# Kernel tuning notes

Hardware: AMD Instinct MI355X
Metric: run time of the kernel (lower is better)

## Reference

```python
import jax, jax.numpy as jnp
import numpy as np

P = 2        # patch size (all 3 dims)
NB = 8       # num_bands
N = 16       # d_state
DTR = 8      # dt_rank = d_model // 16
DCONV = 4    # d_conv
SMAX = 2.0   # smax_dt = smax_B = smax_C


def _ln(x, g, b):
    mu = x.mean(-1, keepdims=True)
    v = ((x - mu) ** 2).mean(-1, keepdims=True)
    return (x - mu) / jnp.sqrt(v + 1e-5) * g + b


def _silu(x):
    return x * jax.nn.sigmoid(x)


def _ssm_layer(x, band, m, rho, Win, bin_, convw, convb, Wx, Wdt, bdt, Alog, Dp,
               Wout, bout, edt, eB, eC, wr, wm):
    # x: [B, L, d_model] -> bidirectional conditioned selective scan (BiFCSSM)
    Bsz, L, _ = x.shape
    ED = convw.shape[0]
    xz = x @ Win + bin_
    xp, z = xz[..., :ED], xz[..., ED:]
    # depthwise causal conv1d over L
    xpad = jnp.pad(xp, ((0, 0), (DCONV - 1, 0), (0, 0)))
    xc = sum(xpad[:, k:k + L, :] * convw[:, k] for k in range(DCONV)) + convb
    xc = _silu(xc)
    dbl = xc @ Wx                                    # [B,L,DTR+2N]
    dt = jax.nn.softplus(dbl[..., :DTR] @ Wdt + bdt)  # [B,L,ED]
    # band/radius/mask conditioned modulation of delta, B, C
    s_dt = SMAX * jax.nn.sigmoid(edt[band][None] + wr[0] * rho[None] + wm[0] * m)
    s_B = SMAX * jax.nn.sigmoid(eB[band][None] + wr[1] * rho[None] + wm[1] * m)
    s_C = SMAX * jax.nn.sigmoid(eC[band][None] + wr[2] * rho[None] + wm[2] * m)
    dt = dt * s_dt[..., None]
    Bm = dbl[..., DTR:DTR + N] * s_B[..., None]       # [B,L,N]
    Cm = dbl[..., DTR + N:] * s_C[..., None]          # [B,L,N]
    A = -jnp.exp(Alog)                                # [ED,N]
    dA = jnp.exp(dt[..., None] * A)                   # [B,L,ED,N]
    dBu = (dA - 1.0) / A * Bm[:, :, None, :] * xc[..., None]   # exact ZOH
    dA_s = jnp.moveaxis(dA, 1, 0)
    dBu_s = jnp.moveaxis(dBu, 1, 0)
    C_s = jnp.moveaxis(Cm, 1, 0)
    h0 = jnp.zeros((Bsz, ED, N), x.dtype)

    def step(h, inp):
        a, bu, c = inp
        h = a * h + bu
        return h, jnp.einsum('ben,bn->be', h, c)

    _, yf = jax.lax.scan(step, h0, (dA_s, dBu_s, C_s))
    _, yb = jax.lax.scan(step, h0, (dA_s, dBu_s, C_s), reverse=True)
    y = jnp.moveaxis(yf + yb, 0, 1) + Dp * xc
    y = y * _silu(z)
    return y @ Wout + bout


def _fwd(kspace_ri, mask, pe_w, pe_b, pu_w, pu_b, ln_g, ln_b, fn_g, fn_b,
         cond_band, cond_rad_w, cond_mask_w, l0_Win, l0_bin, l0_convw, l0_convb,
         l0_Wx, l0_Wdt, l0_bdt, l0_Alog, l0_D, l0_Wout, l0_bout, l0_edt, l0_eB,
         l0_eC, l0_wr, l0_wm):
    Bsz, C, nx, ny, nz = kspace_ri.shape
    gx, gy, gz = nx // P, ny // P, nz // P
    L = gx * gy * gz
    # patch embed (Conv3d, kernel==stride) as blocked einsum
    xr = kspace_ri.reshape(Bsz, C, gx, P, gy, P, gz, P)
    x = jnp.einsum('bcxiyjzk,dcijk->bdxyz', xr, pe_w) + pe_b[None, :, None, None, None]
    DM = x.shape[1]
    x = x.reshape(Bsz, DM, L).transpose(0, 2, 1)               # [B,L,D]
    m = mask.reshape(Bsz, 1, gx, P, gy, P, gz, P).mean(axis=(3, 5, 7)).reshape(Bsz, L)
    m = jnp.clip(m, 0.0, 1.0)
    # raster scan ordering: identity permutation, rho_bar, band ids
    rho = jnp.arange(L, dtype=x.dtype) / float(L - 1)
    band = jnp.clip(jnp.floor(rho * NB).astype(jnp.int32), 0, NB - 1)
    # condition tokens
    cond = cond_band[band][None] + rho[None, :, None] * cond_rad_w + m[:, :, None] * cond_mask_w
    h = _ln(x + cond, ln_g, ln_b)
    h = h + _ssm_layer(_ln(h, fn_g, fn_b), band, m, rho, l0_Win, l0_bin, l0_convw,
                       l0_convb, l0_Wx, l0_Wdt, l0_bdt, l0_Alog, l0_D, l0_Wout,
                       l0_bout, l0_edt, l0_eB, l0_eC, l0_wr, l0_wm)
    # patch unembed (ConvTranspose3d, kernel==stride) as blocked einsum
    hg = h.transpose(0, 2, 1).reshape(Bsz, DM, gx, gy, gz)
    out = jnp.einsum('bdxyz,dcijk->bcxiyjzk', hg, pu_w).reshape(Bsz, C, nx, ny, nz)
    out = out + pu_b[None, :, None, None, None]
    return kspace_ri + out


def setup_inputs() -> dict:
    key = jax.random.key(0)
    ks = jax.random.split(key, 24)
    ED, DM, CIN = 256, 128, 16

    def nrm(k, shape, s):
        return jax.random.normal(k, shape, jnp.float32) * s

    return {
        'kspace_ri': jax.random.normal(ks[0], (1, CIN, 64, 64, 16), jnp.float32),
        'mask': jax.random.uniform(ks[1], (1, 1, 64, 64, 16), jnp.float32),
        'pe_w': nrm(ks[2], (DM, CIN, P, P, P), 0.09),
        'pe_b': nrm(ks[3], (DM,), 0.02),
        'pu_w': nrm(ks[4], (DM, CIN, P, P, P), 0.05),
        'pu_b': jnp.zeros((CIN,), jnp.float32),
        'ln_g': jnp.ones((DM,), jnp.float32),
        'ln_b': jnp.zeros((DM,), jnp.float32),
        'fn_g': jnp.ones((DM,), jnp.float32),
        'fn_b': jnp.zeros((DM,), jnp.float32),
        'cond_band': nrm(ks[5], (NB, DM), 0.02),
        'cond_rad_w': nrm(ks[6], (DM,), 0.02),
        'cond_mask_w': nrm(ks[7], (DM,), 0.02),
        'l0_Win': nrm(ks[8], (DM, 2 * ED), 0.05),
        'l0_bin': jnp.zeros((2 * ED,), jnp.float32),
        'l0_convw': nrm(ks[9], (ED, DCONV), 0.2),
        'l0_convb': jnp.zeros((ED,), jnp.float32),
        'l0_Wx': nrm(ks[10], (ED, DTR + 2 * N), 0.05),
        'l0_Wdt': nrm(ks[11], (DTR, ED), 0.1),
        'l0_bdt': jnp.full((ED,), -3.0, jnp.float32),
        'l0_Alog': jnp.log(jnp.tile(jnp.arange(1, N + 1, dtype=jnp.float32), (ED, 1))),
        'l0_D': jnp.ones((ED,), jnp.float32),
        'l0_Wout': nrm(ks[12], (ED, DM), 0.05),
        'l0_bout': jnp.zeros((DM,), jnp.float32),
        'l0_edt': nrm(ks[13], (NB,), 0.1),
        'l0_eB': nrm(ks[14], (NB,), 0.1),
        'l0_eC': nrm(ks[15], (NB,), 0.1),
        'l0_wr': nrm(ks[16], (3,), 0.1),
        'l0_wm': nrm(ks[17], (3,), 0.1),
    }


def reference(kspace_ri, mask, pe_w, pe_b, pu_w, pu_b, ln_g, ln_b, fn_g, fn_b,
              cond_band, cond_rad_w, cond_mask_w, l0_Win, l0_bin, l0_convw,
              l0_convb, l0_Wx, l0_Wdt, l0_bdt, l0_Alog, l0_D, l0_Wout, l0_bout,
              l0_edt, l0_eB, l0_eC, l0_wr, l0_wm):
    return _fwd(kspace_ri, mask, pe_w, pe_b, pu_w, pu_b, ln_g, ln_b, fn_g, fn_b,
                cond_band, cond_rad_w, cond_mask_w, l0_Win, l0_bin, l0_convw,
                l0_convb, l0_Wx, l0_Wdt, l0_bdt, l0_Alog, l0_D, l0_Wout, l0_bout,
                l0_edt, l0_eB, l0_eC, l0_wr, l0_wm)
```

## Files before the change

### kernel.cpp

```cpp
#include <hip/hip_runtime.h>
#include <hip/hip_bf16.h>

#define L_TOK 8192
#define NCh 256
#define CLh 32
#define LOG2E 1.44269504088896f

typedef short bf16x8 __attribute__((ext_vector_type(8)));
typedef float f32x4 __attribute__((ext_vector_type(4)));

static __device__ __forceinline__ float nexp2(float x) {
#if __has_builtin(__builtin_amdgcn_exp2f)
    return __builtin_amdgcn_exp2f(x);
#else
    return exp2f(x);
#endif
}
static __device__ __forceinline__ float sigm(float x) {
    return 1.f / (1.f + nexp2(-x * LOG2E));
}
static __device__ __forceinline__ ushort f2bf(float x) {
    union { float f; uint u; } v; v.f = x;
    uint r = v.u + 0x7fffu + ((v.u >> 16) & 1u);
    return (ushort)(r >> 16);
}
static __device__ __forceinline__ float bf2f(ushort h) {
    union { float f; uint u; } v; v.u = ((uint)h) << 16;
    return v.f;
}
static __device__ __forceinline__ void f2hl(float x, ushort* hi, ushort* lo) {
    ushort h = f2bf(x);
    *hi = h;
    *lo = f2bf(x - bf2f(h));
}

#define W_PE   0
#define W_WIN  16384
#define W_WOUT 81920
#define W_PU   114688
#define W_PROJ 131072
#define W_TOT  212992

__global__ __launch_bounds__(256) void prep_k(const float* __restrict__ pe_w, const float* __restrict__ Win,
                                              const float* __restrict__ Wx, const float* __restrict__ Wdt,
                                              const float* __restrict__ Wout, const float* __restrict__ pu_w,
                                              const float* __restrict__ mask,
                                              ushort* __restrict__ wH, ushort* __restrict__ wL,
                                              float* __restrict__ mbuf) {
    int b = blockIdx.x;
    if (b >= 832) {
        int l = (b - 832) * 256 + threadIdx.x;
        int xg = l >> 8, yg = (l >> 3) & 31, zg = l & 7;
        float s = 0.f;
        for (int i2 = 0; i2 < 2; ++i2)
            for (int j2 = 0; j2 < 2; ++j2)
                for (int k2 = 0; k2 < 2; ++k2)
                    s += mask[(2 * xg + i2) * 1024 + (2 * yg + j2) * 16 + 2 * zg + k2];
        s *= 0.125f;
        mbuf[l] = fminf(fmaxf(s, 0.f), 1.f);
        return;
    }
    int i = b * 256 + threadIdx.x;
    float v;
    if (i < 16384) {
        v = pe_w[i];
    } else if (i < 81920) {
        int j = i - 16384; int n = j >> 7, k = j & 127;
        v = Win[k * 512 + n];
    } else if (i < 114688) {
        int j = i - 81920; int n = j >> 8, k = j & 255;
        v = Wout[k * 128 + n];
    } else if (i < 131072) {
        int j = i - 114688; int n = j >> 7, k = j & 127;
        v = pu_w[k * 128 + n];
    } else {
        int j = i - 131072; int n = j >> 8, k = j & 255;
        if (n < 256) {
            float s = 0.f;
#pragma unroll
            for (int r = 0; r < 8; ++r) s += Wx[k * 40 + r] * Wdt[r * 256 + n];
            v = s;
        } else if (n < 288) {
            v = Wx[k * 40 + 8 + (n - 256)];
        } else {
            v = 0.f;
        }
    }
    ushort h, lo; f2hl(v, &h, &lo);
    wH[i] = h; wL[i] = lo;
}

__global__ __launch_bounds__(256) void embed_ln_k(const float* __restrict__ ks,
                                                  const ushort* __restrict__ wH, const ushort* __restrict__ wL,
                                                  const float* __restrict__ pe_b, const float* __restrict__ cond_band,
                                                  const float* __restrict__ cond_rad, const float* __restrict__ cond_mask,
                                                  const float* __restrict__ mbuf,
                                                  const float* __restrict__ ln_g, const float* __restrict__ ln_b,
                                                  const float* __restrict__ fn_g, const float* __restrict__ fn_b,
                                                  float* __restrict__ h_,
                                                  ushort* __restrict__ hnH, ushort* __restrict__ hnL) {
    __shared__ __align__(16) char smem[41472];
    ushort (*AsH)[72] = (ushort(*)[72])(smem);
    ushort (*AsL)[72] = (ushort(*)[72])(smem + 2304);
    ushort (*BsH)[72] = (ushort(*)[72])(smem + 4608);
    ushort (*BsL)[72] = (ushort(*)[72])(smem + 23040);
    float  (*Cs)[132] = (float(*)[132])(smem);

    const int tid = threadIdx.x;
    const int lane = tid & 63, wn = tid >> 6;
    const int ln = lane & 15, q = lane >> 4;
    const int mb = blockIdx.x * 16;

    f32x4 acc[2];
    acc[0] = (f32x4){0.f, 0.f, 0.f, 0.f};
    acc[1] = (f32x4){0.f, 0.f, 0.f, 0.f};

    for (int kc = 0; kc < 128; kc += 64) {
        __syncthreads();
        for (int u = tid; u < 1024; u += 256) {
            int r = u >> 6, kk = u & 63;
            int l = mb + r, k = kc + kk;
            int cc = k >> 3, ijk = k & 7;
            int xg = l >> 8, yg = (l >> 3) & 31, zg = l & 7;
            int i2 = (ijk >> 2) & 1, j2 = (ijk >> 1) & 1, k2 = ijk & 1;
            float v = ks[cc * 65536 + (2 * xg + i2) * 1024 + (2 * yg + j2) * 16 + 2 * zg + k2];
            ushort h, lo; f2hl(v, &h, &lo);
            AsH[r][kk] = h; AsL[r][kk] = lo;
        }
        for (int u = tid; u < 1024; u += 256) {
            int n = u >> 3, g = u & 7;
            *(uint4*)&BsH[n][g * 8] = *(const uint4*)&wH[W_PE + n * 128 + kc + g * 8];
            *(uint4*)&BsL[n][g * 8] = *(const uint4*)&wL[W_PE + n * 128 + kc + g * 8];
        }
        __syncthreads();
#pragma unroll
        for (int ks_ = 0; ks_ < 64; ks_ += 32) {
            const int kk = ks_ + q * 8;
            bf16x8 ah = *(const bf16x8*)&AsH[ln][kk];
            bf16x8 al = *(const bf16x8*)&AsL[ln][kk];
#pragma unroll
            for (int cb = 0; cb < 2; ++cb) {
                bf16x8 bh = *(const bf16x8*)&BsH[wn * 32 + cb * 16 + ln][kk];
                bf16x8 bl = *(const bf16x8*)&BsL[wn * 32 + cb * 16 + ln][kk];
                acc[cb] = __builtin_amdgcn_mfma_f32_16x16x32_bf16(ah, bh, acc[cb], 0, 0, 0);
                acc[cb] = __builtin_amdgcn_mfma_f32_16x16x32_bf16(ah, bl, acc[cb], 0, 0, 0);
                acc[cb] = __builtin_amdgcn_mfma_f32_16x16x32_bf16(al, bh, acc[cb], 0, 0, 0);
            }
        }
    }
    __syncthreads();
#pragma unroll
    for (int cb = 0; cb < 2; ++cb) {
#pragma unroll
        for (int r = 0; r < 4; ++r) {
            int row = q * 4 + r;
            int col = wn * 32 + cb * 16 + ln;
            int l = mb + row;
            float rho = (float)l * (1.0f / 8191.0f);
            int band = min(7, (int)(rho * 8.0f));
            Cs[row][col] = acc[cb][r] + pe_b[col] + cond_band[band * 128 + col]
                           + rho * cond_rad[col] + mbuf[l] * cond_mask[col];
        }
    }
    __syncthreads();
    {
        int row = tid >> 4, j = tid & 15;
        int l = mb + row;
        float v8[8];
        float s = 0.f, s2 = 0.f;
#pragma unroll
        for (int i = 0; i < 8; ++i) {
            float v = Cs[row][j * 8 + i];
            v8[i] = v; s += v; s2 += v * v;
        }
#pragma unroll
        for (int o = 1; o < 16; o <<= 1) { s += __shfl_xor(s, o, 16); s2 += __shfl_xor(s2, o, 16); }
        float mu = s * (1.f / 128.f);
        float var = s2 * (1.f / 128.f) - mu * mu;
        float rstd = rsqrtf(fmaxf(var, 0.f) + 1e-5f);
        float hv[8];
        s = 0.f; s2 = 0.f;
#pragma unroll
        for (int i = 0; i < 8; ++i) {
            int col = j * 8 + i;
            float h = (v8[i] - mu) * rstd * ln_g[col] + ln_b[col];
            hv[i] = h; s += h; s2 += h * h;
        }
#pragma unroll
        for (int i = 0; i < 8; i += 4)
            *(float4*)&h_[(size_t)l * 128 + j * 8 + i] = make_float4(hv[i], hv[i + 1], hv[i + 2], hv[i + 3]);
#pragma unroll
        for (int o = 1; o < 16; o <<= 1) { s += __shfl_xor(s, o, 16); s2 += __shfl_xor(s2, o, 16); }
        mu = s * (1.f / 128.f);
        var = s2 * (1.f / 128.f) - mu * mu;
        rstd = rsqrtf(fmaxf(var, 0.f) + 1e-5f);
        union { ushort u[8]; uint4 v4; } oh, ol;
#pragma unroll
        for (int i = 0; i < 8; ++i) {
            int col = j * 8 + i;
            float o2 = (hv[i] - mu) * rstd * fn_g[col] + fn_b[col];
            ushort hh, ll; f2hl(o2, &hh, &ll);
            oh.u[i] = hh; ol.u[i] = ll;
        }
        *(uint4*)&hnH[(size_t)l * 128 + j * 8] = oh.v4;
        *(uint4*)&hnL[(size_t)l * 128 + j * 8] = ol.v4;
    }
}

__global__ __launch_bounds__(256) void win_k(const ushort* __restrict__ Ah, const ushort* __restrict__ Al,
                                             const ushort* __restrict__ wH, const ushort* __restrict__ wL,
                                             const float* __restrict__ bin_,
                                             float* __restrict__ xp, float* __restrict__ sz) {
    __shared__ ushort AsH[64][72], AsL[64][72];
    __shared__ ushort BsH[64][72], BsL[64][72];
    const int tid = threadIdx.x;
    const int lane = tid & 63, wave = tid >> 6;
    const int wm = wave & 1, wn = wave >> 1;
    const int ln = lane & 15, q = lane >> 4;
    const int mb = blockIdx.x * 64, nb = blockIdx.y * 64;

    f32x4 acc[2][2];
#pragma unroll
    for (int rb = 0; rb < 2; ++rb)
#pragma unroll
        for (int cb = 0; cb < 2; ++cb) acc[rb][cb] = (f32x4){0.f, 0.f, 0.f, 0.f};

    for (int kc = 0; kc < 128; kc += 64) {
        __syncthreads();
        for (int u = tid; u < 512; u += 256) {
            int r = u >> 3, g = u & 7;
            size_t go = (size_t)(mb + r) * 128 + kc + g * 8;
            *(uint4*)&AsH[r][g * 8] = *(const uint4*)&Ah[go];
            *(uint4*)&AsL[r][g * 8] = *(const uint4*)&Al[go];
        }
        for (int u = tid; u < 512; u += 256) {
            int n = u >> 3, g = u & 7;
            size_t go = (size_t)(W_WIN) + (size_t)(nb + n) * 128 + kc + g * 8;
            *(uint4*)&BsH[n][g * 8] = *(const uint4*)&wH[go];
            *(uint4*)&BsL[n][g * 8] = *(const uint4*)&wL[go];
        }
        __syncthreads();
#pragma unroll
        for (int ks_ = 0; ks_ < 64; ks_ += 32) {
            const int kk = ks_ + q * 8;
            bf16x8 ah[2], al[2], bh[2], bl[2];
#pragma unroll
            for (int rb = 0; rb < 2; ++rb) {
                ah[rb] = *(const bf16x8*)&AsH[wm * 32 + rb * 16 + ln][kk];
                al[rb] = *(const bf16x8*)&AsL[wm * 32 + rb * 16 + ln][kk];
            }
#pragma unroll
            for (int cb = 0; cb < 2; ++cb) {
                bh[cb] = *(const bf16x8*)&BsH[wn * 32 + cb * 16 + ln][kk];
                bl[cb] = *(const bf16x8*)&BsL[wn * 32 + cb * 16 + ln][kk];
            }
#pragma unroll
            for (int rb = 0; rb < 2; ++rb)
#pragma unroll
                for (int cb = 0; cb < 2; ++cb) {
                    acc[rb][cb] = __builtin_amdgcn_mfma_f32_16x16x32_bf16(ah[rb], bh[cb], acc[rb][cb], 0, 0, 0);
                    acc[rb][cb] = __builtin_amdgcn_mfma_f32_16x16x32_bf16(ah[rb], bl[cb], acc[rb][cb], 0, 0, 0);
                    acc[rb][cb] = __builtin_amdgcn_mfma_f32_16x16x32_bf16(al[rb], bh[cb], acc[rb][cb], 0, 0, 0);
                }
        }
    }
#pragma unroll
    for (int rb = 0; rb < 2; ++rb)
#pragma unroll
        for (int cb = 0; cb < 2; ++cb)
#pragma unroll
            for (int r = 0; r < 4; ++r) {
                int l = mb + wm * 32 + rb * 16 + q * 4 + r;
                int col = nb + wn * 32 + cb * 16 + ln;
                float v = acc[rb][cb][r] + bin_[col];
                if (col < 256) {
                    xp[(size_t)l * 256 + col] = v;
                } else {
                    sz[(size_t)l * 256 + (col - 256)] = v * sigm(v);
                }
            }
}

__global__ __launch_bounds__(256) void conv_k(const float* __restrict__ xp, const float* __restrict__ convw,
                                              const float* __restrict__ convb, float* __restrict__ xc) {
    int id = blockIdx.x * 256 + threadIdx.x;
    int l = id >> 6, e4 = (id & 63) * 4;
    float4 cw[4];
#pragma unroll
    for (int j = 0; j < 4; ++j) cw[j] = *(const float4*)&convw[(e4 + j) * 4];
    float4 cb = *(const float4*)&convb[e4];
    float o[4] = {cb.x, cb.y, cb.z, cb.w};
#pragma unroll
    for (int k = 0; k < 4; ++k) {
        int lp = l - 3 + k;
        if (lp >= 0) {
            float4 t = *(const float4*)&xp[(size_t)lp * 256 + e4];
            o[0] += t.x * ((const float*)&cw[0])[k];
            o[1] += t.y * ((const float*)&cw[1])[k];
            o[2] += t.z * ((const float*)&cw[2])[k];
            o[3] += t.w * ((const float*)&cw[3])[k];
        }
    }
    float4 r;
    r.x = o[0] * sigm(o[0]);
    r.y = o[1] * sigm(o[1]);
    r.z = o[2] * sigm(o[2]);
    r.w = o[3] * sigm(o[3]);
    *(float4*)&xc[(size_t)l * 256 + e4] = r;
}

__global__ __launch_bounds__(256) void proj_k(const float* __restrict__ xc,
                                              const ushort* __restrict__ wH, const ushort* __restrict__ wL,
                                              const float* __restrict__ bdt, const float* __restrict__ mbuf,
                                              const float* __restrict__ edt, const float* __restrict__ eB,
                                              const float* __restrict__ eC, const float* __restrict__ wr,
                                              const float* __restrict__ wm,
                                              float* __restrict__ dt, float* __restrict__ Bm, float* __restrict__ Cm) {
    __shared__ ushort AsH[64][72], AsL[64][72];
    __shared__ ushort BsH[64][72], BsL[64][72];
    const int tid = threadIdx.x;
    const int lane = tid & 63, wave = tid >> 6;
    const int wm_ = wave & 1, wn = wave >> 1;
    const int ln = lane & 15, q = lane >> 4;
    const int mb = blockIdx.x * 64, nb = blockIdx.y * 64;

    f32x4 acc[2][2];
#pragma unroll
    for (int rb = 0; rb < 2; ++rb)
#pragma unroll
        for (int cb = 0; cb < 2; ++cb) acc[rb][cb] = (f32x4){0.f, 0.f, 0.f, 0.f};

    for (int kc = 0; kc < 256; kc += 64) {
        __syncthreads();
        for (int u = tid; u < 1024; u += 256) {
            int r = u >> 4, kq = u & 15;
            float4 v = *(const float4*)&xc[(size_t)(mb + r) * 256 + kc + kq * 4];
            union { ushort u[4]; uint2 v2; } hh, ll;
            f2hl(v.x, &hh.u[0], &ll.u[0]); f2hl(v.y, &hh.u[1], &ll.u[1]);
            f2hl(v.z, &hh.u[2], &ll.u[2]); f2hl(v.w, &hh.u[3], &ll.u[3]);
            *(uint2*)&AsH[r][kq * 4] = hh.v2;
            *(uint2*)&AsL[r][kq * 4] = ll.v2;
        }
        for (int u = tid; u < 512; u += 256) {
            int n = u >> 3, g = u & 7;
            size_t go = (size_t)(W_PROJ) + (size_t)(nb + n) * 256 + kc + g * 8;
            *(uint4*)&BsH[n][g * 8] = *(const uint4*)&wH[go];
            *(uint4*)&BsL[n][g * 8] = *(const uint4*)&wL[go];
        }
        __syncthreads();
#pragma unroll
        for (int ks_ = 0; ks_ < 64; ks_ += 32) {
            const int kk = ks_ + q * 8;
            bf16x8 ah[2], al[2], bh[2], bl[2];
#pragma unroll
            for (int rb = 0; rb < 2; ++rb) {
                ah[rb] = *(const bf16x8*)&AsH[wm_ * 32 + rb * 16 + ln][kk];
                al[rb] = *(const bf16x8*)&AsL[wm_ * 32 + rb * 16 + ln][kk];
            }
#pragma unroll
            for (int cb = 0; cb < 2; ++cb) {
                bh[cb] = *(const bf16x8*)&BsH[wn * 32 + cb * 16 + ln][kk];
                bl[cb] = *(const bf16x8*)&BsL[wn * 32 + cb * 16 + ln][kk];
            }
#pragma unroll
            for (int rb = 0; rb < 2; ++rb)
#pragma unroll
                for (int cb = 0; cb < 2; ++cb) {
                    acc[rb][cb] = __builtin_amdgcn_mfma_f32_16x16x32_bf16(ah[rb], bh[cb], acc[rb][cb], 0, 0, 0);
                    acc[rb][cb] = __builtin_amdgcn_mfma_f32_16x16x32_bf16(ah[rb], bl[cb], acc[rb][cb], 0, 0, 0);
                    acc[rb][cb] = __builtin_amdgcn_mfma_f32_16x16x32_bf16(al[rb], bh[cb], acc[rb][cb], 0, 0, 0);
                }
        }
    }
#pragma unroll
    for (int rb = 0; rb < 2; ++rb)
#pragma unroll
        for (int cb = 0; cb < 2; ++cb)
#pragma unroll
            for (int r = 0; r < 4; ++r) {
                int l = mb + wm_ * 32 + rb * 16 + q * 4 + r;
                int col = nb + wn * 32 + cb * 16 + ln;
                float v = acc[rb][cb][r];
                float rho = (float)l * (1.0f / 8191.0f);
                int band = min(7, (int)(rho * 8.0f));
                float mv = mbuf[l];
                if (col < 256) {
                    float sc0 = 2.0f * sigm(edt[band] + wr[0] * rho + wm[0] * mv);
                    float v2 = v + bdt[col];
                    float sp = (v2 > 20.f) ? v2 : log1pf(expf(v2));
                    dt[(size_t)l * 256 + col] = sp * sc0;
                } else if (col < 272) {
                    float sc1 = 2.0f * sigm(eB[band] + wr[1] * rho + wm[1] * mv);
                    Bm[(size_t)l * 16 + (col - 256)] = v * sc1;
                } else if (col < 288) {
                    float sc2 = 2.0f * sigm(eC[band] + wr[2] * rho + wm[2] * mv);
                    Cm[(size_t)l * 16 + (col - 272)] = v * sc2;
                }
            }
}

__global__ __launch_bounds__(256) void scan0_k(const float* __restrict__ dt, const float* __restrict__ xc,
                                               const float* __restrict__ Bm, const float* __restrict__ Alog,
                                               float* __restrict__ Hb, float* __restrict__ sdtb) {
    const int c = blockIdx.x, dir = blockIdx.y, e = threadIdx.x;
    __shared__ float bms[CLh][16];
    for (int idx = e; idx < CLh * 16; idx += 256)
        bms[idx >> 4][idx & 15] = Bm[c * (CLh * 16) + idx];
    float A2[16], iv[16], h[16];
#pragma unroll
    for (int n = 0; n < 16; ++n) {
        float ea = nexp2(Alog[e * 16 + n] * LOG2E);
        A2[n] = -ea * LOG2E;
        iv[n] = -1.0f / ea;
        h[n] = 0.f;
    }
    const int base = c * CLh;
    float cu[8], cx[8], nu[8], nx[8];
#pragma unroll
    for (int j = 0; j < 8; ++j) {
        int p = dir ? (CLh - 1 - j) : j;
        cu[j] = dt[(size_t)(base + p) * 256 + e];
        cx[j] = xc[(size_t)(base + p) * 256 + e];
    }
    __syncthreads();
    float sdt = 0.f;
#pragma unroll
    for (int g = 0; g < CLh / 8; ++g) {
        if (g + 1 < CLh / 8) {
#pragma unroll
            for (int j = 0; j < 8; ++j) {
                int s = (g + 1) * 8 + j;
                int p = dir ? (CLh - 1 - s) : s;
                nu[j] = dt[(size_t)(base + p) * 256 + e];
                nx[j] = xc[(size_t)(base + p) * 256 + e];
            }
        }
#pragma unroll
        for (int j = 0; j < 8; ++j) {
            int s = g * 8 + j;
            int p = dir ? (CLh - 1 - s) : s;
            float u = cu[j], xv = cx[j];
            union { float4 v[4]; float f[16]; } bb;
            const float4* bp = (const float4*)&bms[p][0];
            bb.v[0] = bp[0]; bb.v[1] = bp[1]; bb.v[2] = bp[2]; bb.v[3] = bp[3];
#pragma unroll
            for (int n = 0; n < 16; ++n) {
                float a = nexp2(A2[n] * u);
                float w = xv * bb.f[n] * iv[n];
                h[n] = a * (h[n] + w) - w;
            }
            sdt += u;
        }
#pragma unroll
        for (int j = 0; j < 8; ++j) { cu[j] = nu[j]; cx[j] = nx[j]; }
    }
    const size_t hofs = (size_t)(dir * NCh + c) * 4096 + e * 16;
#pragma unroll
    for (int j = 0; j < 4; ++j)
        *(float4*)&Hb[hofs + 4 * j] = make_float4(h[4 * j], h[4 * j + 1], h[4 * j + 2], h[4 * j + 3]);
    if (dir == 0) sdtb[c * 256 + e] = sdt;
}

__global__ __launch_bounds__(64) void combine_k(const float* __restrict__ Hb, float* __restrict__ Hpre,
                                                const float* __restrict__ sdtb, const float* __restrict__ Alog) {
    int id = blockIdx.x * 64 + threadIdx.x;
    int dir = id >> 12, en = id & 4095, e = en >> 4;
    float A2 = -nexp2(Alog[en] * LOG2E) * LOG2E;
    float hi = 0.f;
    for (int g = 0; g < NCh / 8; ++g) {
        float Pv[8], qv[8];
#pragma unroll
        for (int j = 0; j < 8; ++j) {
            int c = dir ? (NCh - 1 - (g * 8 + j)) : (g * 8 + j);
            Pv[j] = sdtb[c * 256 + e];
            qv[j] = Hb[(size_t)(dir * NCh + c) * 4096 + en];
        }
#pragma unroll
        for (int j = 0; j < 8; ++j) {
            int c = dir ? (NCh - 1 - (g * 8 + j)) : (g * 8 + j);
            float P = nexp2(A2 * Pv[j]);
            Hpre[(size_t)(dir * NCh + c) * 4096 + en] = hi;
            hi = P * hi + qv[j];
        }
    }
}

template <int DIR>
static __device__ __forceinline__ void scan_dir(const float* __restrict__ dt, const float* __restrict__ xc,
                                                int base, int e,
                                                const float (*bms)[16], const float (*cms)[16],
                                                const float* A2, const float* iv,
                                                float* h, float* yreg) {
    float cu[8], cx[8], nu[8], nx[8];
#pragma unroll
    for (int j = 0; j < 8; ++j) {
        const int p = DIR ? (CLh - 1 - j) : j;
        cu[j] = dt[(size_t)(base + p) * 256 + e];
        cx[j] = xc[(size_t)(base + p) * 256 + e];
    }
#pragma unroll
    for (int g = 0; g < CLh / 8; ++g) {
        if (g + 1 < CLh / 8) {
#pragma unroll
            for (int j = 0; j < 8; ++j) {
                const int s = (g + 1) * 8 + j;
                const int p = DIR ? (CLh - 1 - s) : s;
                nu[j] = dt[(size_t)(base + p) * 256 + e];
                nx[j] = xc[(size_t)(base + p) * 256 + e];
            }
        }
#pragma unroll
        for (int j = 0; j < 8; ++j) {
            const int s = g * 8 + j;
            const int p = DIR ? (CLh - 1 - s) : s;
            float u = cu[j], xv = cx[j];
            union { float4 v[4]; float f[16]; } bb, cc;
            const float4* bp = (const float4*)&bms[p][0];
            bb.v[0] = bp[0]; bb.v[1] = bp[1]; bb.v[2] = bp[2]; bb.v[3] = bp[3];
            const float4* cp = (const float4*)&cms[p][0];
            cc.v[0] = cp[0]; cc.v[1] = cp[1]; cc.v[2] = cp[2]; cc.v[3] = cp[3];
            float y = 0.f;
#pragma unroll
            for (int n = 0; n < 16; ++n) {
                float a = nexp2(A2[n] * u);
                float w = xv * bb.f[n] * iv[n];
                h[n] = a * (h[n] + w) - w;
                y += h[n] * cc.f[n];
            }
            yreg[p] = y;
        }
#pragma unroll
        for (int j = 0; j < 8; ++j) { cu[j] = nu[j]; cx[j] = nx[j]; }
    }
}

__global__ __launch_bounds__(512) void scan1g_k(const float* __restrict__ dt, const float* __restrict__ xc,
                                                const float* __restrict__ Bm, const float* __restrict__ Cm,
                                                const float* __restrict__ Alog, const float* __restrict__ Hpre,
                                                const float* __restrict__ sz, const float* __restrict__ Dp,
                                                ushort* __restrict__ AHo, ushort* __restrict__ ALo) {
    const int c = blockIdx.x;
    const int tid = threadIdx.x;
    const int dir = tid >> 8;
    const int e = tid & 255;
    __shared__ float bms[CLh][16];
    __shared__ float cms[CLh][16];
    __shared__ float ysum[CLh][256];
    for (int idx = tid; idx < CLh * 16; idx += 512) {
        bms[idx >> 4][idx & 15] = Bm[c * (CLh * 16) + idx];
        cms[idx >> 4][idx & 15] = Cm[c * (CLh * 16) + idx];
    }
    float A2[16], iv[16], h[16];
#pragma unroll
    for (int n = 0; n < 16; ++n) {
        float ea = nexp2(Alog[e * 16 + n] * LOG2E);
        A2[n] = -ea * LOG2E;
        iv[n] = -1.0f / ea;
    }
    const size_t hofs = (size_t)(dir * NCh + c) * 4096 + e * 16;
#pragma unroll
    for (int j = 0; j < 4; ++j) {
        float4 hv = *(const float4*)&Hpre[hofs + 4 * j];
        h[4 * j] = hv.x; h[4 * j + 1] = hv.y; h[4 * j + 2] = hv.z; h[4 * j + 3] = hv.w;
    }
    const int base = c * CLh;
    float yreg[CLh];
    __syncthreads();
    if (dir == 0) {
        scan_dir<0>(dt, xc, base, e, bms, cms, A2, iv, h, yreg);
    } else {
        scan_dir<1>(dt, xc, base, e, bms, cms, A2, iv, h, yreg);
    }
    __syncthreads();
    if (dir == 0) {
#pragma unroll
        for (int l = 0; l < CLh; ++l) ysum[l][e] = yreg[l];
    }
    __syncthreads();
    if (dir == 1) {
        float dpv = Dp[e];
#pragma unroll
        for (int l = 0; l < CLh; ++l) {
            size_t gl = (size_t)(base + l) * 256 + e;
            float a = (ysum[l][e] + yreg[l] + dpv * xc[gl]) * sz[gl];
            ushort hh, ll; f2hl(a, &hh, &ll);
            AHo[gl] = hh; ALo[gl] = ll;
        }
    }
}

__global__ __launch_bounds__(256) void wout_k(const ushort* __restrict__ AH, const ushort* __restrict__ AL,
                                              const ushort* __restrict__ wH, const ushort* __restrict__ wL,
                                              const float* __restrict__ bout, const float* __restrict__ h_,
                                              ushort* __restrict__ hfH, ushort* __restrict__ hfL) {
    __shared__ ushort AsH[32][72], AsL[32][72];
    __shared__ ushort BsH[64][72], BsL[64][72];
    const int tid = threadIdx.x;
    const int lane = tid & 63, wave = tid >> 6;
    const int wm = wave & 1, wn = wave >> 1;
    const int ln = lane & 15, q = lane >> 4;
    const int mb = blockIdx.x * 32, nb = blockIdx.y * 64;

    f32x4 acc[2];
    acc[0] = (f32x4){0.f, 0.f, 0.f, 0.f};
    acc[1] = (f32x4){0.f, 0.f, 0.f, 0.f};

    for (int kc = 0; kc < 256; kc += 64) {
        __syncthreads();
        for (int u = tid; u < 256; u += 256) {
            int r = u >> 3, g = u & 7;
            size_t go = (size_t)(mb + r) * 256 + kc + g * 8;
            *(uint4*)&AsH[r][g * 8] = *(const uint4*)&AH[go];
            *(uint4*)&AsL[r][g * 8] = *(const uint4*)&AL[go];
        }
        for (int u = tid; u < 512; u += 256) {
            int n = u >> 3, g = u & 7;
            size_t go = (size_t)(W_WOUT) + (size_t)(nb + n) * 256 + kc + g * 8;
            *(uint4*)&BsH[n][g * 8] = *(const uint4*)&wH[go];
            *(uint4*)&BsL[n][g * 8] = *(const uint4*)&wL[go];
        }
        __syncthreads();
#pragma unroll
        for (int ks_ = 0; ks_ < 64; ks_ += 32) {
            const int kk = ks_ + q * 8;
            bf16x8 ah = *(const bf16x8*)&AsH[wm * 16 + ln][kk];
            bf16x8 al = *(const bf16x8*)&AsL[wm * 16 + ln][kk];
#pragma unroll
            for (int cb = 0; cb < 2; ++cb) {
                bf16x8 bh = *(const bf16x8*)&BsH[wn * 32 + cb * 16 + ln][kk];
                bf16x8 bl = *(const bf16x8*)&BsL[wn * 32 + cb * 16 + ln][kk];
                acc[cb] = __builtin_amdgcn_mfma_f32_16x16x32_bf16(ah, bh, acc[cb], 0, 0, 0);
                acc[cb] = __builtin_amdgcn_mfma_f32_16x16x32_bf16(ah, bl, acc[cb], 0, 0, 0);
                acc[cb] = __builtin_amdgcn_mfma_f32_16x16x32_bf16(al, bh, acc[cb], 0, 0, 0);
            }
        }
    }
#pragma unroll
    for (int cb = 0; cb < 2; ++cb)
#pragma unroll
        for (int r = 0; r < 4; ++r) {
            int l = mb + wm * 16 + q * 4 + r;
            int col = nb + wn * 32 + cb * 16 + ln;
            float v = acc[cb][r] + bout[col] + h_[(size_t)l * 128 + col];
            ushort hh, ll; f2hl(v, &hh, &ll);
            hfH[(size_t)l * 128 + col] = hh;
            hfL[(size_t)l * 128 + col] = ll;
        }
}

__global__ __launch_bounds__(256) void unembed_k(const ushort* __restrict__ Ah, const ushort* __restrict__ Al,
                                                 const ushort* __restrict__ wH, const ushort* __restrict__ wL,
                                                 const float* __restrict__ pu_b, const float* __restrict__ ks,
                                                 float* __restrict__ out) {
    __shared__ ushort AsH[32][72], AsL[32][72];
    __shared__ ushort BsH[64][72], BsL[64][72];
    const int tid = threadIdx.x;
    const int lane = tid & 63, wave = tid >> 6;
    const int wm = wave & 1, wn = wave >> 1;
    const int ln = lane & 15, q = lane >> 4;
    const int mb = blockIdx.x * 32, nb = blockIdx.y * 64;

    f32x4 acc[2];
    acc[0] = (f32x4){0.f, 0.f, 0.f, 0.f};
    acc[1] = (f32x4){0.f, 0.f, 0.f, 0.f};

    for (int kc = 0; kc < 128; kc += 64) {
        __syncthreads();
        for (int u = tid; u < 256; u += 256) {
            int r = u >> 3, g = u & 7;
            size_t go = (size_t)(mb + r) * 128 + kc + g * 8;
            *(uint4*)&AsH[r][g * 8] = *(const uint4*)&Ah[go];
            *(uint4*)&AsL[r][g * 8] = *(const uint4*)&Al[go];
        }
        for (int u = tid; u < 512; u += 256) {
            int n = u >> 3, g = u & 7;
            size_t go = (size_t)(W_PU) + (size_t)(nb + n) * 128 + kc + g * 8;
            *(uint4*)&BsH[n][g * 8] = *(const uint4*)&wH[go];
            *(uint4*)&BsL[n][g * 8] = *(const uint4*)&wL[go];
        }
        __syncthreads();
#pragma unroll
        for (int ks_ = 0; ks_ < 64; ks_ += 32) {
            const int kk = ks_ + q * 8;
            bf16x8 ah = *(const bf16x8*)&AsH[wm * 16 + ln][kk];
            bf16x8 al = *(const bf16x8*)&AsL[wm * 16 + ln][kk];
#pragma unroll
            for (int cb = 0; cb < 2; ++cb) {
                bf16x8 bh = *(const bf16x8*)&BsH[wn * 32 + cb * 16 + ln][kk];
                bf16x8 bl = *(const bf16x8*)&BsL[wn * 32 + cb * 16 + ln][kk];
                acc[cb] = __builtin_amdgcn_mfma_f32_16x16x32_bf16(ah, bh, acc[cb], 0, 0, 0);
                acc[cb] = __builtin_amdgcn_mfma_f32_16x16x32_bf16(ah, bl, acc[cb], 0, 0, 0);
                acc[cb] = __builtin_amdgcn_mfma_f32_16x16x32_bf16(al, bh, acc[cb], 0, 0, 0);
            }
        }
    }
#pragma unroll
    for (int cb = 0; cb < 2; ++cb)
#pragma unroll
        for (int r = 0; r < 4; ++r) {
            int l = mb + wm * 16 + q * 4 + r;
            int col = nb + wn * 32 + cb * 16 + ln;
            int xg = l >> 8, yg = (l >> 3) & 31, zg = l & 7;
            int c = col >> 3, ijk = col & 7;
            int i2 = (ijk >> 2) & 1, j2 = (ijk >> 1) & 1, k2 = ijk & 1;
            size_t idx = (size_t)((c * 64 + 2 * xg + i2) * 64 + (2 * yg + j2)) * 16 + 2 * zg + k2;
            out[idx] = acc[cb][r] + pu_b[c] + ks[idx];
        }
}

extern "C" void kernel_launch(void* const* d_in, const int* in_sizes, int n_in,
                              void* d_out, int out_size, void* d_ws, size_t ws_size,
                              hipStream_t stream) {
    const float* ks    = (const float*)d_in[0];
    const float* mask  = (const float*)d_in[1];
    const float* pe_w  = (const float*)d_in[2];
    const float* pe_b  = (const float*)d_in[3];
    const float* pu_w  = (const float*)d_in[4];
    const float* pu_b  = (const float*)d_in[5];
    const float* ln_g  = (const float*)d_in[6];
    const float* ln_b  = (const float*)d_in[7];
    const float* fn_g  = (const float*)d_in[8];
    const float* fn_b  = (const float*)d_in[9];
    const float* cond_band = (const float*)d_in[10];
    const float* cond_rad  = (const float*)d_in[11];
    const float* cond_mask = (const float*)d_in[12];
    const float* Win   = (const float*)d_in[13];
    const float* bin_  = (const float*)d_in[14];
    const float* convw = (const float*)d_in[15];
    const float* convb = (const float*)d_in[16];
    const float* Wx    = (const float*)d_in[17];
    const float* Wdt   = (const float*)d_in[18];
    const float* bdt   = (const float*)d_in[19];
    const float* Alog  = (const float*)d_in[20];
    const float* Dp    = (const float*)d_in[21];
    const float* Wout  = (const float*)d_in[22];
    const float* bout  = (const float*)d_in[23];
    const float* edt   = (const float*)d_in[24];
    const float* eB    = (const float*)d_in[25];
    const float* eC    = (const float*)d_in[26];
    const float* wr    = (const float*)d_in[27];
    const float* wm    = (const float*)d_in[28];
    float* out = (float*)d_out;

    char* base = (char*)d_ws;
    size_t o = 0;
    auto alloc = [&](size_t bytes) { char* p = base + o; o += (bytes + 255) & ~(size_t)255; return p; };
    float*  mbuf = (float*)alloc(32768);
    ushort* wH   = (ushort*)alloc(W_TOT * 2);
    ushort* wL   = (ushort*)alloc(W_TOT * 2);
    float*  h_   = (float*)alloc(4194304);
    ushort* hnH  = (ushort*)alloc(2097152);
    ushort* hnL  = (ushort*)alloc(2097152);
    float*  xp   = (float*)alloc(8388608);
    float*  sz   = (float*)alloc(8388608);
    float*  xc   = (float*)alloc(8388608);
    float*  dt   = (float*)alloc(8388608);
    float*  Bm   = (float*)alloc(524288);
    float*  Cm   = (float*)alloc(524288);
    float*  Hb   = (float*)alloc(8388608);
    float*  Hpre = (float*)alloc(8388608);
    float*  sdtb = (float*)alloc(262144);
    ushort* AHo  = (ushort*)alloc(4194304);
    ushort* ALo  = (ushort*)alloc(4194304);
    ushort* hfH  = (ushort*)alloc(2097152);
    ushort* hfL  = (ushort*)alloc(2097152);

    prep_k<<<864, 256, 0, stream>>>(pe_w, Win, Wx, Wdt, Wout, pu_w, mask, wH, wL, mbuf);
    embed_ln_k<<<512, 256, 0, stream>>>(ks, wH, wL, pe_b, cond_band, cond_rad, cond_mask, mbuf,
                                        ln_g, ln_b, fn_g, fn_b, h_, hnH, hnL);
    win_k<<<dim3(128, 8), 256, 0, stream>>>(hnH, hnL, wH, wL, bin_, xp, sz);
    conv_k<<<2048, 256, 0, stream>>>(xp, convw, convb, xc);
    proj_k<<<dim3(128, 5), 256, 0, stream>>>(xc, wH, wL, bdt, mbuf, edt, eB, eC, wr, wm, dt, Bm, Cm);
    scan0_k<<<dim3(NCh, 2), 256, 0, stream>>>(dt, xc, Bm, Alog, Hb, sdtb);
    combine_k<<<128, 64, 0, stream>>>(Hb, Hpre, sdtb, Alog);
    scan1g_k<<<NCh, 512, 0, stream>>>(dt, xc, Bm, Cm, Alog, Hpre, sz, Dp, AHo, ALo);
    wout_k<<<dim3(256, 2), 256, 0, stream>>>(AHo, ALo, wH, wL, bout, h_, hfH, hfL);
    unembed_k<<<dim3(256, 2), 256, 0, stream>>>(hfH, hfL, wH, wL, pu_b, ks, out);
}
```

Measured before the change: 240.0 us.

## Fuse all pipeline stages into one cooperative persistent megakernel with grid syncs

Replaces the ten separate kernel launches (prep, embed+LN, in-projection, conv, projection, two-pass chunked scan, combine, out-projection, unembed) with a single cooperative kernel of 256 blocks × 512 threads that separates stages with grid-wide syncs. The aim is to remove per-launch overhead and inter-kernel gaps. In exchange, every stage is forced onto a fixed 256-block, 512-thread configuration, which may lower occupancy or parallelism for stages that previously used larger grids. Grid syncs also add their own barrier cost.

```diff
diff --git a/kernel.cpp b/kernel.cpp
--- a/kernel.cpp
+++ b/kernel.cpp
@@ -1,7 +1,8 @@
 #include <hip/hip_runtime.h>
 #include <hip/hip_bf16.h>
-
-#define L_TOK 8192
+#include <hip/hip_cooperative_groups.h>
+namespace cg = cooperative_groups;
+
 #define NCh 256
 #define CLh 32
 #define LOG2E 1.44269504088896f
@@ -41,449 +42,17 @@
 #define W_PROJ 131072
 #define W_TOT  212992
 
-__global__ __launch_bounds__(256) void prep_k(const float* __restrict__ pe_w, const float* __restrict__ Win,
-                                              const float* __restrict__ Wx, const float* __restrict__ Wdt,
-                                              const float* __restrict__ Wout, const float* __restrict__ pu_w,
-                                              const float* __restrict__ mask,
-                                              ushort* __restrict__ wH, ushort* __restrict__ wL,
-                                              float* __restrict__ mbuf) {
-    int b = blockIdx.x;
-    if (b >= 832) {
-        int l = (b - 832) * 256 + threadIdx.x;
-        int xg = l >> 8, yg = (l >> 3) & 31, zg = l & 7;
-        float s = 0.f;
-        for (int i2 = 0; i2 < 2; ++i2)
-            for (int j2 = 0; j2 < 2; ++j2)
-                for (int k2 = 0; k2 < 2; ++k2)
-                    s += mask[(2 * xg + i2) * 1024 + (2 * yg + j2) * 16 + 2 * zg + k2];
-        s *= 0.125f;
-        mbuf[l] = fminf(fmaxf(s, 0.f), 1.f);
-        return;
-    }
-    int i = b * 256 + threadIdx.x;
-    float v;
-    if (i < 16384) {
-        v = pe_w[i];
-    } else if (i < 81920) {
-        int j = i - 16384; int n = j >> 7, k = j & 127;
-        v = Win[k * 512 + n];
-    } else if (i < 114688) {
-        int j = i - 81920; int n = j >> 8, k = j & 255;
-        v = Wout[k * 128 + n];
-    } else if (i < 131072) {
-        int j = i - 114688; int n = j >> 7, k = j & 127;
-        v = pu_w[k * 128 + n];
-    } else {
-        int j = i - 131072; int n = j >> 8, k = j & 255;
-        if (n < 256) {
-            float s = 0.f;
-#pragma unroll
-            for (int r = 0; r < 8; ++r) s += Wx[k * 40 + r] * Wdt[r * 256 + n];
-            v = s;
-        } else if (n < 288) {
-            v = Wx[k * 40 + 8 + (n - 256)];
-        } else {
-            v = 0.f;
-        }
-    }
-    ushort h, lo; f2hl(v, &h, &lo);
-    wH[i] = h; wL[i] = lo;
-}
-
-__global__ __launch_bounds__(256) void embed_ln_k(const float* __restrict__ ks,
-                                                  const ushort* __restrict__ wH, const ushort* __restrict__ wL,
-                                                  const float* __restrict__ pe_b, const float* __restrict__ cond_band,
-                                                  const float* __restrict__ cond_rad, const float* __restrict__ cond_mask,
-                                                  const float* __restrict__ mbuf,
-                                                  const float* __restrict__ ln_g, const float* __restrict__ ln_b,
-                                                  const float* __restrict__ fn_g, const float* __restrict__ fn_b,
-                                                  float* __restrict__ h_,
-                                                  ushort* __restrict__ hnH, ushort* __restrict__ hnL) {
-    __shared__ __align__(16) char smem[41472];
-    ushort (*AsH)[72] = (ushort(*)[72])(smem);
-    ushort (*AsL)[72] = (ushort(*)[72])(smem + 2304);
-    ushort (*BsH)[72] = (ushort(*)[72])(smem + 4608);
-    ushort (*BsL)[72] = (ushort(*)[72])(smem + 23040);
-    float  (*Cs)[132] = (float(*)[132])(smem);
-
-    const int tid = threadIdx.x;
-    const int lane = tid & 63, wn = tid >> 6;
-    const int ln = lane & 15, q = lane >> 4;
-    const int mb = blockIdx.x * 16;
-
-    f32x4 acc[2];
-    acc[0] = (f32x4){0.f, 0.f, 0.f, 0.f};
-    acc[1] = (f32x4){0.f, 0.f, 0.f, 0.f};
-
-    for (int kc = 0; kc < 128; kc += 64) {
-        __syncthreads();
-        for (int u = tid; u < 1024; u += 256) {
-            int r = u >> 6, kk = u & 63;
-            int l = mb + r, k = kc + kk;
-            int cc = k >> 3, ijk = k & 7;
-            int xg = l >> 8, yg = (l >> 3) & 31, zg = l & 7;
-            int i2 = (ijk >> 2) & 1, j2 = (ijk >> 1) & 1, k2 = ijk & 1;
-            float v = ks[cc * 65536 + (2 * xg + i2) * 1024 + (2 * yg + j2) * 16 + 2 * zg + k2];
-            ushort h, lo; f2hl(v, &h, &lo);
-            AsH[r][kk] = h; AsL[r][kk] = lo;
-        }
-        for (int u = tid; u < 1024; u += 256) {
-            int n = u >> 3, g = u & 7;
-            *(uint4*)&BsH[n][g * 8] = *(const uint4*)&wH[W_PE + n * 128 + kc + g * 8];
-            *(uint4*)&BsL[n][g * 8] = *(const uint4*)&wL[W_PE + n * 128 + kc + g * 8];
-        }
-        __syncthreads();
-#pragma unroll
-        for (int ks_ = 0; ks_ < 64; ks_ += 32) {
-            const int kk = ks_ + q * 8;
-            bf16x8 ah = *(const bf16x8*)&AsH[ln][kk];
-            bf16x8 al = *(const bf16x8*)&AsL[ln][kk];
-#pragma unroll
-            for (int cb = 0; cb < 2; ++cb) {
-                bf16x8 bh = *(const bf16x8*)&BsH[wn * 32 + cb * 16 + ln][kk];
-                bf16x8 bl = *(const bf16x8*)&BsL[wn * 32 + cb * 16 + ln][kk];
-                acc[cb] = __builtin_amdgcn_mfma_f32_16x16x32_bf16(ah, bh, acc[cb], 0, 0, 0);
-                acc[cb] = __builtin_amdgcn_mfma_f32_16x16x32_bf16(ah, bl, acc[cb], 0, 0, 0);
-                acc[cb] = __builtin_amdgcn_mfma_f32_16x16x32_bf16(al, bh, acc[cb], 0, 0, 0);
-            }
-        }
-    }
-    __syncthreads();
-#pragma unroll
-    for (int cb = 0; cb < 2; ++cb) {
-#pragma unroll
-        for (int r = 0; r < 4; ++r) {
-            int row = q * 4 + r;
-            int col = wn * 32 + cb * 16 + ln;
-            int l = mb + row;
-            float rho = (float)l * (1.0f / 8191.0f);
-            int band = min(7, (int)(rho * 8.0f));
-            Cs[row][col] = acc[cb][r] + pe_b[col] + cond_band[band * 128 + col]
-                           + rho * cond_rad[col] + mbuf[l] * cond_mask[col];
-        }
-    }
-    __syncthreads();
-    {
-        int row = tid >> 4, j = tid & 15;
-        int l = mb + row;
-        float v8[8];
-        float s = 0.f, s2 = 0.f;
-#pragma unroll
-        for (int i = 0; i < 8; ++i) {
-            float v = Cs[row][j * 8 + i];
-            v8[i] = v; s += v; s2 += v * v;
-        }
-#pragma unroll
-        for (int o = 1; o < 16; o <<= 1) { s += __shfl_xor(s, o, 16); s2 += __shfl_xor(s2, o, 16); }
-        float mu = s * (1.f / 128.f);
-        float var = s2 * (1.f / 128.f) - mu * mu;
-        float rstd = rsqrtf(fmaxf(var, 0.f) + 1e-5f);
-        float hv[8];
-        s = 0.f; s2 = 0.f;
-#pragma unroll
-        for (int i = 0; i < 8; ++i) {
-            int col = j * 8 + i;
-            float h = (v8[i] - mu) * rstd * ln_g[col] + ln_b[col];
-            hv[i] = h; s += h; s2 += h * h;
-        }
-#pragma unroll
-        for (int i = 0; i < 8; i += 4)
-            *(float4*)&h_[(size_t)l * 128 + j * 8 + i] = make_float4(hv[i], hv[i + 1], hv[i + 2], hv[i + 3]);
-#pragma unroll
-        for (int o = 1; o < 16; o <<= 1) { s += __shfl_xor(s, o, 16); s2 += __shfl_xor(s2, o, 16); }
-        mu = s * (1.f / 128.f);
-        var = s2 * (1.f / 128.f) - mu * mu;
-        rstd = rsqrtf(fmaxf(var, 0.f) + 1e-5f);
-        union { ushort u[8]; uint4 v4; } oh, ol;
-#pragma unroll
-        for (int i = 0; i < 8; ++i) {
-            int col = j * 8 + i;
-            float o2 = (hv[i] - mu) * rstd * fn_g[col] + fn_b[col];
-            ushort hh, ll; f2hl(o2, &hh, &ll);
-            oh.u[i] = hh; ol.u[i] = ll;
-        }
-        *(uint4*)&hnH[(size_t)l * 128 + j * 8] = oh.v4;
-        *(uint4*)&hnL[(size_t)l * 128 + j * 8] = ol.v4;
-    }
-}
-
-__global__ __launch_bounds__(256) void win_k(const ushort* __restrict__ Ah, const ushort* __restrict__ Al,
-                                             const ushort* __restrict__ wH, const ushort* __restrict__ wL,
-                                             const float* __restrict__ bin_,
-                                             float* __restrict__ xp, float* __restrict__ sz) {
-    __shared__ ushort AsH[64][72], AsL[64][72];
-    __shared__ ushort BsH[64][72], BsL[64][72];
-    const int tid = threadIdx.x;
-    const int lane = tid & 63, wave = tid >> 6;
-    const int wm = wave & 1, wn = wave >> 1;
-    const int ln = lane & 15, q = lane >> 4;
-    const int mb = blockIdx.x * 64, nb = blockIdx.y * 64;
-
-    f32x4 acc[2][2];
-#pragma unroll
-    for (int rb = 0; rb < 2; ++rb)
-#pragma unroll
-        for (int cb = 0; cb < 2; ++cb) acc[rb][cb] = (f32x4){0.f, 0.f, 0.f, 0.f};
-
-    for (int kc = 0; kc < 128; kc += 64) {
-        __syncthreads();
-        for (int u = tid; u < 512; u += 256) {
-            int r = u >> 3, g = u & 7;
-            size_t go = (size_t)(mb + r) * 128 + kc + g * 8;
-            *(uint4*)&AsH[r][g * 8] = *(const uint4*)&Ah[go];
-            *(uint4*)&AsL[r][g * 8] = *(const uint4*)&Al[go];
-        }
-        for (int u = tid; u < 512; u += 256) {
-            int n = u >> 3, g = u & 7;
-            size_t go = (size_t)(W_WIN) + (size_t)(nb + n) * 128 + kc + g * 8;
-            *(uint4*)&BsH[n][g * 8] = *(const uint4*)&wH[go];
-            *(uint4*)&BsL[n][g * 8] = *(const uint4*)&wL[go];
-        }
-        __syncthreads();
-#pragma unroll
-        for (int ks_ = 0; ks_ < 64; ks_ += 32) {
-            const int kk = ks_ + q * 8;
-            bf16x8 ah[2], al[2], bh[2], bl[2];
-#pragma unroll
-            for (int rb = 0; rb < 2; ++rb) {
-                ah[rb] = *(const bf16x8*)&AsH[wm * 32 + rb * 16 + ln][kk];
-                al[rb] = *(const bf16x8*)&AsL[wm * 32 + rb * 16 + ln][kk];
-            }
-#pragma unroll
-            for (int cb = 0; cb < 2; ++cb) {
-                bh[cb] = *(const bf16x8*)&BsH[wn * 32 + cb * 16 + ln][kk];
-                bl[cb] = *(const bf16x8*)&BsL[wn * 32 + cb * 16 + ln][kk];
-            }
-#pragma unroll
-            for (int rb = 0; rb < 2; ++rb)
-#pragma unroll
-                for (int cb = 0; cb < 2; ++cb) {
-                    acc[rb][cb] = __builtin_amdgcn_mfma_f32_16x16x32_bf16(ah[rb], bh[cb], acc[rb][cb], 0, 0, 0);
-                    acc[rb][cb] = __builtin_amdgcn_mfma_f32_16x16x32_bf16(ah[rb], bl[cb], acc[rb][cb], 0, 0, 0);
-                    acc[rb][cb] = __builtin_amdgcn_mfma_f32_16x16x32_bf16(al[rb], bh[cb], acc[rb][cb], 0, 0, 0);
-                }
-        }
-    }
-#pragma unroll
-    for (int rb = 0; rb < 2; ++rb)
-#pragma unroll
-        for (int cb = 0; cb < 2; ++cb)
-#pragma unroll
-            for (int r = 0; r < 4; ++r) {
-                int l = mb + wm * 32 + rb * 16 + q * 4 + r;
-                int col = nb + wn * 32 + cb * 16 + ln;
-                float v = acc[rb][cb][r] + bin_[col];
-                if (col < 256) {
-                    xp[(size_t)l * 256 + col] = v;
-                } else {
-                    sz[(size_t)l * 256 + (col - 256)] = v * sigm(v);
-                }
-            }
-}
-
-__global__ __launch_bounds__(256) void conv_k(const float* __restrict__ xp, const float* __restrict__ convw,
-                                              const float* __restrict__ convb, float* __restrict__ xc) {
-    int id = blockIdx.x * 256 + threadIdx.x;
-    int l = id >> 6, e4 = (id & 63) * 4;
-    float4 cw[4];
-#pragma unroll
-    for (int j = 0; j < 4; ++j) cw[j] = *(const float4*)&convw[(e4 + j) * 4];
-    float4 cb = *(const float4*)&convb[e4];
-    float o[4] = {cb.x, cb.y, cb.z, cb.w};
-#pragma unroll
-    for (int k = 0; k < 4; ++k) {
-        int lp = l - 3 + k;
-        if (lp >= 0) {
-            float4 t = *(const float4*)&xp[(size_t)lp * 256 + e4];
-            o[0] += t.x * ((const float*)&cw[0])[k];
-            o[1] += t.y * ((const float*)&cw[1])[k];
-            o[2] += t.z * ((const float*)&cw[2])[k];
-            o[3] += t.w * ((const float*)&cw[3])[k];
-        }
-    }
-    float4 r;
-    r.x = o[0] * sigm(o[0]);
-    r.y = o[1] * sigm(o[1]);
-    r.z = o[2] * sigm(o[2]);
-    r.w = o[3] * sigm(o[3]);
-    *(float4*)&xc[(size_t)l * 256 + e4] = r;
-}
-
-__global__ __launch_bounds__(256) void proj_k(const float* __restrict__ xc,
-                                              const ushort* __restrict__ wH, const ushort* __restrict__ wL,
-                                              const float* __restrict__ bdt, const float* __restrict__ mbuf,
-                                              const float* __restrict__ edt, const float* __restrict__ eB,
-                                              const float* __restrict__ eC, const float* __restrict__ wr,
-                                              const float* __restrict__ wm,
-                                              float* __restrict__ dt, float* __restrict__ Bm, float* __restrict__ Cm) {
-    __shared__ ushort AsH[64][72], AsL[64][72];
-    __shared__ ushort BsH[64][72], BsL[64][72];
-    const int tid = threadIdx.x;
-    const int lane = tid & 63, wave = tid >> 6;
-    const int wm_ = wave & 1, wn = wave >> 1;
-    const int ln = lane & 15, q = lane >> 4;
-    const int mb = blockIdx.x * 64, nb = blockIdx.y * 64;
-
-    f32x4 acc[2][2];
-#pragma unroll
-    for (int rb = 0; rb < 2; ++rb)
-#pragma unroll
-        for (int cb = 0; cb < 2; ++cb) acc[rb][cb] = (f32x4){0.f, 0.f, 0.f, 0.f};
-
-    for (int kc = 0; kc < 256; kc += 64) {
-        __syncthreads();
-        for (int u = tid; u < 1024; u += 256) {
-            int r = u >> 4, kq = u & 15;
-            float4 v = *(const float4*)&xc[(size_t)(mb + r) * 256 + kc + kq * 4];
-            union { ushort u[4]; uint2 v2; } hh, ll;
-            f2hl(v.x, &hh.u[0], &ll.u[0]); f2hl(v.y, &hh.u[1], &ll.u[1]);
-            f2hl(v.z, &hh.u[2], &ll.u[2]); f2hl(v.w, &hh.u[3], &ll.u[3]);
-            *(uint2*)&AsH[r][kq * 4] = hh.v2;
-            *(uint2*)&AsL[r][kq * 4] = ll.v2;
-        }
-        for (int u = tid; u < 512; u += 256) {
-            int n = u >> 3, g = u & 7;
-            size_t go = (size_t)(W_PROJ) + (size_t)(nb + n) * 256 + kc + g * 8;
-            *(uint4*)&BsH[n][g * 8] = *(const uint4*)&wH[go];
-            *(uint4*)&BsL[n][g * 8] = *(const uint4*)&wL[go];
-        }
-        __syncthreads();
-#pragma unroll
-        for (int ks_ = 0; ks_ < 64; ks_ += 32) {
-            const int kk = ks_ + q * 8;
-            bf16x8 ah[2], al[2], bh[2], bl[2];
-#pragma unroll
-            for (int rb = 0; rb < 2; ++rb) {
-                ah[rb] = *(const bf16x8*)&AsH[wm_ * 32 + rb * 16 + ln][kk];
-                al[rb] = *(const bf16x8*)&AsL[wm_ * 32 + rb * 16 + ln][kk];
-            }
-#pragma unroll
-            for (int cb = 0; cb < 2; ++cb) {
-                bh[cb] = *(const bf16x8*)&BsH[wn * 32 + cb * 16 + ln][kk];
-                bl[cb] = *(const bf16x8*)&BsL[wn * 32 + cb * 16 + ln][kk];
-            }
-#pragma unroll
-            for (int rb = 0; rb < 2; ++rb)
-#pragma unroll
-                for (int cb = 0; cb < 2; ++cb) {
-                    acc[rb][cb] = __builtin_amdgcn_mfma_f32_16x16x32_bf16(ah[rb], bh[cb], acc[rb][cb], 0, 0, 0);
-                    acc[rb][cb] = __builtin_amdgcn_mfma_f32_16x16x32_bf16(ah[rb], bl[cb], acc[rb][cb], 0, 0, 0);
-                    acc[rb][cb] = __builtin_amdgcn_mfma_f32_16x16x32_bf16(al[rb], bh[cb], acc[rb][cb], 0, 0, 0);
-                }
-        }
-    }
-#pragma unroll
-    for (int rb = 0; rb < 2; ++rb)
-#pragma unroll
-        for (int cb = 0; cb < 2; ++cb)
-#pragma unroll
-            for (int r = 0; r < 4; ++r) {
-                int l = mb + wm_ * 32 + rb * 16 + q * 4 + r;
-                int col = nb + wn * 32 + cb * 16 + ln;
-                float v = acc[rb][cb][r];
-                float rho = (float)l * (1.0f / 8191.0f);
-                int band = min(7, (int)(rho * 8.0f));
-                float mv = mbuf[l];
-                if (col < 256) {
-                    float sc0 = 2.0f * sigm(edt[band] + wr[0] * rho + wm[0] * mv);
-                    float v2 = v + bdt[col];
-                    float sp = (v2 > 20.f) ? v2 : log1pf(expf(v2));
-                    dt[(size_t)l * 256 + col] = sp * sc0;
-                } else if (col < 272) {
-                    float sc1 = 2.0f * sigm(eB[band] + wr[1] * rho + wm[1] * mv);
-                    Bm[(size_t)l * 16 + (col - 256)] = v * sc1;
-                } else if (col < 288) {
-                    float sc2 = 2.0f * sigm(eC[band] + wr[2] * rho + wm[2] * mv);
-                    Cm[(size_t)l * 16 + (col - 272)] = v * sc2;
-                }
-            }
-}
-
-__global__ __launch_bounds__(256) void scan0_k(const float* __restrict__ dt, const float* __restrict__ xc,
-                                               const float* __restrict__ Bm, const float* __restrict__ Alog,
-                                               float* __restrict__ Hb, float* __restrict__ sdtb) {
-    const int c = blockIdx.x, dir = blockIdx.y, e = threadIdx.x;
-    __shared__ float bms[CLh][16];
-    for (int idx = e; idx < CLh * 16; idx += 256)
-        bms[idx >> 4][idx & 15] = Bm[c * (CLh * 16) + idx];
-    float A2[16], iv[16], h[16];
-#pragma unroll
-    for (int n = 0; n < 16; ++n) {
-        float ea = nexp2(Alog[e * 16 + n] * LOG2E);
-        A2[n] = -ea * LOG2E;
-        iv[n] = -1.0f / ea;
-        h[n] = 0.f;
-    }
-    const int base = c * CLh;
-    float cu[8], cx[8], nu[8], nx[8];
-#pragma unroll
-    for (int j = 0; j < 8; ++j) {
-        int p = dir ? (CLh - 1 - j) : j;
-        cu[j] = dt[(size_t)(base + p) * 256 + e];
-        cx[j] = xc[(size_t)(base + p) * 256 + e];
-    }
-    __syncthreads();
-    float sdt = 0.f;
-#pragma unroll
-    for (int g = 0; g < CLh / 8; ++g) {
-        if (g + 1 < CLh / 8) {
-#pragma unroll
-            for (int j = 0; j < 8; ++j) {
-                int s = (g + 1) * 8 + j;
-                int p = dir ? (CLh - 1 - s) : s;
-                nu[j] = dt[(size_t)(base + p) * 256 + e];
-                nx[j] = xc[(size_t)(base + p) * 256 + e];
-            }
-        }
-#pragma unroll
-        for (int j = 0; j < 8; ++j) {
-            int s = g * 8 + j;
-            int p = dir ? (CLh - 1 - s) : s;
-            float u = cu[j], xv = cx[j];
-            union { float4 v[4]; float f[16]; } bb;
-            const float4* bp = (const float4*)&bms[p][0];
-            bb.v[0] = bp[0]; bb.v[1] = bp[1]; bb.v[2] = bp[2]; bb.v[3] = bp[3];
-#pragma unroll
-            for (int n = 0; n < 16; ++n) {
-                float a = nexp2(A2[n] * u);
-                float w = xv * bb.f[n] * iv[n];
-                h[n] = a * (h[n] + w) - w;
-            }
-            sdt += u;
-        }
-#pragma unroll
-        for (int j = 0; j < 8; ++j) { cu[j] = nu[j]; cx[j] = nx[j]; }
-    }
-    const size_t hofs = (size_t)(dir * NCh + c) * 4096 + e * 16;
-#pragma unroll
-    for (int j = 0; j < 4; ++j)
-        *(float4*)&Hb[hofs + 4 * j] = make_float4(h[4 * j], h[4 * j + 1], h[4 * j + 2], h[4 * j + 3]);
-    if (dir == 0) sdtb[c * 256 + e] = sdt;
-}
-
-__global__ __launch_bounds__(64) void combine_k(const float* __restrict__ Hb, float* __restrict__ Hpre,
-                                                const float* __restrict__ sdtb, const float* __restrict__ Alog) {
-    int id = blockIdx.x * 64 + threadIdx.x;
-    int dir = id >> 12, en = id & 4095, e = en >> 4;
-    float A2 = -nexp2(Alog[en] * LOG2E) * LOG2E;
-    float hi = 0.f;
-    for (int g = 0; g < NCh / 8; ++g) {
-        float Pv[8], qv[8];
-#pragma unroll
-        for (int j = 0; j < 8; ++j) {
-            int c = dir ? (NCh - 1 - (g * 8 + j)) : (g * 8 + j);
-            Pv[j] = sdtb[c * 256 + e];
-            qv[j] = Hb[(size_t)(dir * NCh + c) * 4096 + en];
-        }
-#pragma unroll
-        for (int j = 0; j < 8; ++j) {
-            int c = dir ? (NCh - 1 - (g * 8 + j)) : (g * 8 + j);
-            float P = nexp2(A2 * Pv[j]);
-            Hpre[(size_t)(dir * NCh + c) * 4096 + en] = hi;
-            hi = P * hi + qv[j];
-        }
-    }
-}
+struct KParams {
+    const float *ks, *mask, *pe_w, *pe_b, *pu_w, *pu_b, *ln_g, *ln_b, *fn_g, *fn_b;
+    const float *cond_band, *cond_rad, *cond_mask, *Win, *bin_, *convw, *convb, *Wx, *Wdt, *bdt;
+    const float *Alog, *Dp, *Wout, *bout, *edt, *eB, *eC, *wr, *wm;
+    ushort *wH, *wL;
+    float *mbuf, *h_;
+    ushort *hnH, *hnL;
+    float *xp, *sz, *xc, *dt, *Bm, *Cm, *Hb, *Hpre, *sdtb;
+    ushort *AHo, *ALo, *hfH, *hfL;
+    float *out;
+};
 
 template <int DIR>
 static __device__ __forceinline__ void scan_dir(const float* __restrict__ dt, const float* __restrict__ xc,
@@ -534,246 +103,644 @@
     }
 }
 
-__global__ __launch_bounds__(512) void scan1g_k(const float* __restrict__ dt, const float* __restrict__ xc,
-                                                const float* __restrict__ Bm, const float* __restrict__ Cm,
-                                                const float* __restrict__ Alog, const float* __restrict__ Hpre,
-                                                const float* __restrict__ sz, const float* __restrict__ Dp,
-                                                ushort* __restrict__ AHo, ushort* __restrict__ ALo) {
-    const int c = blockIdx.x;
+__global__ __launch_bounds__(512) void mega_k(KParams P) {
+    cg::grid_group gg = cg::this_grid();
+    __shared__ __align__(16) char smem[55296];
     const int tid = threadIdx.x;
-    const int dir = tid >> 8;
-    const int e = tid & 255;
-    __shared__ float bms[CLh][16];
-    __shared__ float cms[CLh][16];
-    __shared__ float ysum[CLh][256];
-    for (int idx = tid; idx < CLh * 16; idx += 512) {
-        bms[idx >> 4][idx & 15] = Bm[c * (CLh * 16) + idx];
-        cms[idx >> 4][idx & 15] = Cm[c * (CLh * 16) + idx];
-    }
-    float A2[16], iv[16], h[16];
-#pragma unroll
-    for (int n = 0; n < 16; ++n) {
-        float ea = nexp2(Alog[e * 16 + n] * LOG2E);
-        A2[n] = -ea * LOG2E;
-        iv[n] = -1.0f / ea;
-    }
-    const size_t hofs = (size_t)(dir * NCh + c) * 4096 + e * 16;
-#pragma unroll
-    for (int j = 0; j < 4; ++j) {
-        float4 hv = *(const float4*)&Hpre[hofs + 4 * j];
-        h[4 * j] = hv.x; h[4 * j + 1] = hv.y; h[4 * j + 2] = hv.z; h[4 * j + 3] = hv.w;
-    }
-    const int base = c * CLh;
-    float yreg[CLh];
-    __syncthreads();
-    if (dir == 0) {
-        scan_dir<0>(dt, xc, base, e, bms, cms, A2, iv, h, yreg);
-    } else {
-        scan_dir<1>(dt, xc, base, e, bms, cms, A2, iv, h, yreg);
-    }
-    __syncthreads();
-    if (dir == 0) {
-#pragma unroll
-        for (int l = 0; l < CLh; ++l) ysum[l][e] = yreg[l];
-    }
-    __syncthreads();
-    if (dir == 1) {
-        float dpv = Dp[e];
-#pragma unroll
-        for (int l = 0; l < CLh; ++l) {
-            size_t gl = (size_t)(base + l) * 256 + e;
-            float a = (ysum[l][e] + yreg[l] + dpv * xc[gl]) * sz[gl];
-            ushort hh, ll; f2hl(a, &hh, &ll);
-            AHo[gl] = hh; ALo[gl] = ll;
-        }
-    }
-}
-
-__global__ __launch_bounds__(256) void wout_k(const ushort* __restrict__ AH, const ushort* __restrict__ AL,
-                                              const ushort* __restrict__ wH, const ushort* __restrict__ wL,
-                                              const float* __restrict__ bout, const float* __restrict__ h_,
-                                              ushort* __restrict__ hfH, ushort* __restrict__ hfL) {
-    __shared__ ushort AsH[32][72], AsL[32][72];
-    __shared__ ushort BsH[64][72], BsL[64][72];
-    const int tid = threadIdx.x;
-    const int lane = tid & 63, wave = tid >> 6;
-    const int wm = wave & 1, wn = wave >> 1;
-    const int ln = lane & 15, q = lane >> 4;
-    const int mb = blockIdx.x * 32, nb = blockIdx.y * 64;
-
-    f32x4 acc[2];
-    acc[0] = (f32x4){0.f, 0.f, 0.f, 0.f};
-    acc[1] = (f32x4){0.f, 0.f, 0.f, 0.f};
-
-    for (int kc = 0; kc < 256; kc += 64) {
+    const int b = blockIdx.x;
+    const int gtid = b * 512 + tid;
+
+    for (int i = gtid; i < 221184; i += 131072) {
+        if (i < 212992) {
+            float v;
+            if (i < 16384) {
+                v = P.pe_w[i];
+            } else if (i < 81920) {
+                int j = i - 16384; int n = j >> 7, k = j & 127;
+                v = P.Win[k * 512 + n];
+            } else if (i < 114688) {
+                int j = i - 81920; int n = j >> 8, k = j & 255;
+                v = P.Wout[k * 128 + n];
+            } else if (i < 131072) {
+                int j = i - 114688; int n = j >> 7, k = j & 127;
+                v = P.pu_w[k * 128 + n];
+            } else {
+                int j = i - 131072; int n = j >> 8, k = j & 255;
+                if (n < 256) {
+                    float s = 0.f;
+#pragma unroll
+                    for (int r = 0; r < 8; ++r) s += P.Wx[k * 40 + r] * P.Wdt[r * 256 + n];
+                    v = s;
+                } else if (n < 288) {
+                    v = P.Wx[k * 40 + 8 + (n - 256)];
+                } else {
+                    v = 0.f;
+                }
+            }
+            ushort hh, ll; f2hl(v, &hh, &ll);
+            P.wH[i] = hh; P.wL[i] = ll;
+        } else {
+            int l = i - 212992;
+            int xg = l >> 8, yg = (l >> 3) & 31, zg = l & 7;
+            float s = 0.f;
+            for (int i2 = 0; i2 < 2; ++i2)
+                for (int j2 = 0; j2 < 2; ++j2)
+                    for (int k2 = 0; k2 < 2; ++k2)
+                        s += P.mask[(2 * xg + i2) * 1024 + (2 * yg + j2) * 16 + 2 * zg + k2];
+            P.mbuf[l] = fminf(fmaxf(s * 0.125f, 0.f), 1.f);
+        }
+    }
+    gg.sync();
+
+    {
+        ushort (*AsH)[72] = (ushort(*)[72])(smem);
+        ushort (*AsL)[72] = (ushort(*)[72])(smem + 4608);
+        ushort (*BsH)[72] = (ushort(*)[72])(smem + 9216);
+        ushort (*BsL)[72] = (ushort(*)[72])(smem + 27648);
+        float  (*Cs)[132] = (float(*)[132])(smem);
+        const int lane = tid & 63, wv = tid >> 6;
+        const int ln = lane & 15, q = lane >> 4;
+        const int mb = b * 32;
+        f32x4 acc[2];
+        acc[0] = (f32x4){0.f, 0.f, 0.f, 0.f};
+        acc[1] = (f32x4){0.f, 0.f, 0.f, 0.f};
+        for (int kc = 0; kc < 128; kc += 64) {
+            __syncthreads();
+            for (int u = tid; u < 2048; u += 512) {
+                int r = u >> 6, kk = u & 63;
+                int l = mb + r, k = kc + kk;
+                int cc = k >> 3, ijk = k & 7;
+                int xg = l >> 8, yg = (l >> 3) & 31, zg = l & 7;
+                int i2 = (ijk >> 2) & 1, j2 = (ijk >> 1) & 1, k2 = ijk & 1;
+                float v = P.ks[cc * 65536 + (2 * xg + i2) * 1024 + (2 * yg + j2) * 16 + 2 * zg + k2];
+                ushort hh, ll; f2hl(v, &hh, &ll);
+                AsH[r][kk] = hh; AsL[r][kk] = ll;
+            }
+            for (int u = tid; u < 1024; u += 512) {
+                int n = u >> 3, g = u & 7;
+                *(uint4*)&BsH[n][g * 8] = *(const uint4*)&P.wH[W_PE + n * 128 + kc + g * 8];
+                *(uint4*)&BsL[n][g * 8] = *(const uint4*)&P.wL[W_PE + n * 128 + kc + g * 8];
+            }
+            __syncthreads();
+#pragma unroll
+            for (int ks_ = 0; ks_ < 64; ks_ += 32) {
+                const int kk = ks_ + q * 8;
+                bf16x8 bh = *(const bf16x8*)&BsH[wv * 16 + ln][kk];
+                bf16x8 bl = *(const bf16x8*)&BsL[wv * 16 + ln][kk];
+#pragma unroll
+                for (int rb = 0; rb < 2; ++rb) {
+                    bf16x8 ah = *(const bf16x8*)&AsH[rb * 16 + ln][kk];
+                    bf16x8 al = *(const bf16x8*)&AsL[rb * 16 + ln][kk];
+                    acc[rb] = __builtin_amdgcn_mfma_f32_16x16x32_bf16(ah, bh, acc[rb], 0, 0, 0);
+                    acc[rb] = __builtin_amdgcn_mfma_f32_16x16x32_bf16(ah, bl, acc[rb], 0, 0, 0);
+                    acc[rb] = __builtin_amdgcn_mfma_f32_16x16x32_bf16(al, bh, acc[rb], 0, 0, 0);
+                }
+            }
+        }
         __syncthreads();
-        for (int u = tid; u < 256; u += 256) {
-            int r = u >> 3, g = u & 7;
-            size_t go = (size_t)(mb + r) * 256 + kc + g * 8;
-            *(uint4*)&AsH[r][g * 8] = *(const uint4*)&AH[go];
-            *(uint4*)&AsL[r][g * 8] = *(const uint4*)&AL[go];
-        }
-        for (int u = tid; u < 512; u += 256) {
-            int n = u >> 3, g = u & 7;
-            size_t go = (size_t)(W_WOUT) + (size_t)(nb + n) * 256 + kc + g * 8;
-            *(uint4*)&BsH[n][g * 8] = *(const uint4*)&wH[go];
-            *(uint4*)&BsL[n][g * 8] = *(const uint4*)&wL[go];
+#pragma unroll
+        for (int rb = 0; rb < 2; ++rb) {
+#pragma unroll
+            for (int r = 0; r < 4; ++r) {
+                int row = rb * 16 + q * 4 + r;
+                int col = wv * 16 + ln;
+                int l = mb + row;
+                float rho = (float)l * (1.0f / 8191.0f);
+                int band = min(7, (int)(rho * 8.0f));
+                Cs[row][col] = acc[rb][r] + P.pe_b[col] + P.cond_band[band * 128 + col]
+                               + rho * P.cond_rad[col] + P.mbuf[l] * P.cond_mask[col];
+            }
         }
         __syncthreads();
-#pragma unroll
-        for (int ks_ = 0; ks_ < 64; ks_ += 32) {
-            const int kk = ks_ + q * 8;
-            bf16x8 ah = *(const bf16x8*)&AsH[wm * 16 + ln][kk];
-            bf16x8 al = *(const bf16x8*)&AsL[wm * 16 + ln][kk];
-#pragma unroll
-            for (int cb = 0; cb < 2; ++cb) {
-                bf16x8 bh = *(const bf16x8*)&BsH[wn * 32 + cb * 16 + ln][kk];
-                bf16x8 bl = *(const bf16x8*)&BsL[wn * 32 + cb * 16 + ln][kk];
-                acc[cb] = __builtin_amdgcn_mfma_f32_16x16x32_bf16(ah, bh, acc[cb], 0, 0, 0);
-                acc[cb] = __builtin_amdgcn_mfma_f32_16x16x32_bf16(ah, bl, acc[cb], 0, 0, 0);
-                acc[cb] = __builtin_amdgcn_mfma_f32_16x16x32_bf16(al, bh, acc[cb], 0, 0, 0);
-            }
-        }
-    }
-#pragma unroll
-    for (int cb = 0; cb < 2; ++cb)
-#pragma unroll
-        for (int r = 0; r < 4; ++r) {
-            int l = mb + wm * 16 + q * 4 + r;
-            int col = nb + wn * 32 + cb * 16 + ln;
-            float v = acc[cb][r] + bout[col] + h_[(size_t)l * 128 + col];
-            ushort hh, ll; f2hl(v, &hh, &ll);
-            hfH[(size_t)l * 128 + col] = hh;
-            hfL[(size_t)l * 128 + col] = ll;
-        }
-}
-
-__global__ __launch_bounds__(256) void unembed_k(const ushort* __restrict__ Ah, const ushort* __restrict__ Al,
-                                                 const ushort* __restrict__ wH, const ushort* __restrict__ wL,
-                                                 const float* __restrict__ pu_b, const float* __restrict__ ks,
-                                                 float* __restrict__ out) {
-    __shared__ ushort AsH[32][72], AsL[32][72];
-    __shared__ ushort BsH[64][72], BsL[64][72];
-    const int tid = threadIdx.x;
-    const int lane = tid & 63, wave = tid >> 6;
-    const int wm = wave & 1, wn = wave >> 1;
-    const int ln = lane & 15, q = lane >> 4;
-    const int mb = blockIdx.x * 32, nb = blockIdx.y * 64;
-
-    f32x4 acc[2];
-    acc[0] = (f32x4){0.f, 0.f, 0.f, 0.f};
-    acc[1] = (f32x4){0.f, 0.f, 0.f, 0.f};
-
-    for (int kc = 0; kc < 128; kc += 64) {
+        {
+            int row = tid >> 4, j = tid & 15;
+            int l = mb + row;
+            float v8[8];
+            float s = 0.f, s2 = 0.f;
+#pragma unroll
+            for (int i = 0; i < 8; ++i) {
+                float v = Cs[row][j * 8 + i];
+                v8[i] = v; s += v; s2 += v * v;
+            }
+#pragma unroll
+            for (int o = 1; o < 16; o <<= 1) { s += __shfl_xor(s, o, 16); s2 += __shfl_xor(s2, o, 16); }
+            float mu = s * (1.f / 128.f);
+            float var = s2 * (1.f / 128.f) - mu * mu;
+            float rstd = rsqrtf(fmaxf(var, 0.f) + 1e-5f);
+            float hv[8];
+            s = 0.f; s2 = 0.f;
+#pragma unroll
+            for (int i = 0; i < 8; ++i) {
+                int col = j * 8 + i;
+                float h = (v8[i] - mu) * rstd * P.ln_g[col] + P.ln_b[col];
+                hv[i] = h; s += h; s2 += h * h;
+            }
+#pragma unroll
+            for (int i = 0; i < 8; i += 4)
+                *(float4*)&P.h_[(size_t)l * 128 + j * 8 + i] = make_float4(hv[i], hv[i + 1], hv[i + 2], hv[i + 3]);
+#pragma unroll
+            for (int o = 1; o < 16; o <<= 1) { s += __shfl_xor(s, o, 16); s2 += __shfl_xor(s2, o, 16); }
+            mu = s * (1.f / 128.f);
+            var = s2 * (1.f / 128.f) - mu * mu;
+            rstd = rsqrtf(fmaxf(var, 0.f) + 1e-5f);
+            union { ushort u[8]; uint4 v4; } oh, ol;
+#pragma unroll
+            for (int i = 0; i < 8; ++i) {
+                int col = j * 8 + i;
+                float o2 = (hv[i] - mu) * rstd * P.fn_g[col] + P.fn_b[col];
+                ushort hh, ll; f2hl(o2, &hh, &ll);
+                oh.u[i] = hh; ol.u[i] = ll;
+            }
+            *(uint4*)&P.hnH[(size_t)l * 128 + j * 8] = oh.v4;
+            *(uint4*)&P.hnL[(size_t)l * 128 + j * 8] = ol.v4;
+        }
+    }
+    gg.sync();
+
+    {
+        ushort (*AsH)[72] = (ushort(*)[72])(smem);
+        ushort (*AsL)[72] = (ushort(*)[72])(smem + 9216);
+        ushort (*BsH)[72] = (ushort(*)[72])(smem + 18432);
+        ushort (*BsL)[72] = (ushort(*)[72])(smem + 36864);
+        const int lane = tid & 63, wave = tid >> 6;
+        const int wm2 = wave & 1, wn4 = wave >> 1;
+        const int ln = lane & 15, q = lane >> 4;
+        for (int it = 0; it < 2; ++it) {
+            int t = b + it * 256;
+            int mb = (t & 127) * 64, nb = (t >> 7) * 128;
+            f32x4 acc[2][2];
+#pragma unroll
+            for (int rb = 0; rb < 2; ++rb)
+#pragma unroll
+                for (int cb = 0; cb < 2; ++cb) acc[rb][cb] = (f32x4){0.f, 0.f, 0.f, 0.f};
+            for (int kc = 0; kc < 128; kc += 64) {
+                __syncthreads();
+                {
+                    int u = tid;
+                    int r = u >> 3, g = u & 7;
+                    size_t go = (size_t)(mb + r) * 128 + kc + g * 8;
+                    *(uint4*)&AsH[r][g * 8] = *(const uint4*)&P.hnH[go];
+                    *(uint4*)&AsL[r][g * 8] = *(const uint4*)&P.hnL[go];
+                }
+                for (int u = tid; u < 1024; u += 512) {
+                    int n = u >> 3, g = u & 7;
+                    size_t go = (size_t)(W_WIN) + (size_t)(nb + n) * 128 + kc + g * 8;
+                    *(uint4*)&BsH[n][g * 8] = *(const uint4*)&P.wH[go];
+                    *(uint4*)&BsL[n][g * 8] = *(const uint4*)&P.wL[go];
+                }
+                __syncthreads();
+#pragma unroll
+                for (int ks_ = 0; ks_ < 64; ks_ += 32) {
+                    const int kk = ks_ + q * 8;
+                    bf16x8 ah[2], al[2], bh[2], bl[2];
+#pragma unroll
+                    for (int rb = 0; rb < 2; ++rb) {
+                        ah[rb] = *(const bf16x8*)&AsH[wm2 * 32 + rb * 16 + ln][kk];
+                        al[rb] = *(const bf16x8*)&AsL[wm2 * 32 + rb * 16 + ln][kk];
+                    }
+#pragma unroll
+                    for (int cb = 0; cb < 2; ++cb) {
+                        bh[cb] = *(const bf16x8*)&BsH[wn4 * 32 + cb * 16 + ln][kk];
+                        bl[cb] = *(const bf16x8*)&BsL[wn4 * 32 + cb * 16 + ln][kk];
+                    }
+#pragma unroll
+                    for (int rb = 0; rb < 2; ++rb)
+#pragma unroll
+                        for (int cb = 0; cb < 2; ++cb) {
+                            acc[rb][cb] = __builtin_amdgcn_mfma_f32_16x16x32_bf16(ah[rb], bh[cb], acc[rb][cb], 0, 0, 0);
+                            acc[rb][cb] = __builtin_amdgcn_mfma_f32_16x16x32_bf16(ah[rb], bl[cb], acc[rb][cb], 0, 0, 0);
+                            acc[rb][cb] = __builtin_amdgcn_mfma_f32_16x16x32_bf16(al[rb], bh[cb], acc[rb][cb], 0, 0, 0);
+                        }
+                }
+            }
+#pragma unroll
+            for (int rb = 0; rb < 2; ++rb)
+#pragma unroll
+                for (int cb = 0; cb < 2; ++cb)
+#pragma unroll
+                    for (int r = 0; r < 4; ++r) {
+                        int l = mb + wm2 * 32 + rb * 16 + q * 4 + r;
+                        int col = nb + wn4 * 32 + cb * 16 + ln;
+                        float v = acc[rb][cb][r] + P.bin_[col];
+                        if (col < 256) {
+                            P.xp[(size_t)l * 256 + col] = v;
+                        } else {
+                            P.sz[(size_t)l * 256 + (col - 256)] = v * sigm(v);
+                        }
+                    }
+        }
+    }
+    gg.sync();
+
+    for (int id = gtid; id < 524288; id += 131072) {
+        int l = id >> 6, e4 = (id & 63) * 4;
+        float4 cw[4];
+#pragma unroll
+        for (int j = 0; j < 4; ++j) cw[j] = *(const float4*)&P.convw[(e4 + j) * 4];
+        float4 cb = *(const float4*)&P.convb[e4];
+        float o[4] = {cb.x, cb.y, cb.z, cb.w};
+#pragma unroll
+        for (int k = 0; k < 4; ++k) {
+            int lp = l - 3 + k;
+            if (lp >= 0) {
+                float4 t = *(const float4*)&P.xp[(size_t)lp * 256 + e4];
+                o[0] += t.x * ((const float*)&cw[0])[k];
+                o[1] += t.y * ((const float*)&cw[1])[k];
+                o[2] += t.z * ((const float*)&cw[2])[k];
+                o[3] += t.w * ((const float*)&cw[3])[k];
+            }
+        }
+        float4 r;
+        r.x = o[0] * sigm(o[0]);
+        r.y = o[1] * sigm(o[1]);
+        r.z = o[2] * sigm(o[2]);
+        r.w = o[3] * sigm(o[3]);
+        *(float4*)&P.xc[(size_t)l * 256 + e4] = r;
+    }
+    gg.sync();
+
+    {
+        ushort (*AsH)[72] = (ushort(*)[72])(smem);
+        ushort (*AsL)[72] = (ushort(*)[72])(smem + 4608);
+        ushort (*BsH)[72] = (ushort(*)[72])(smem + 9216);
+        ushort (*BsL)[72] = (ushort(*)[72])(smem + 18432);
+        const int lane = tid & 63, wave = tid >> 6;
+        const int wm2 = wave & 1, wn4 = wave >> 1;
+        const int ln = lane & 15, q = lane >> 4;
+        const int mb = b * 32;
+        for (int it = 0; it < 5; ++it) {
+            int nb = it * 64;
+            f32x4 acc = (f32x4){0.f, 0.f, 0.f, 0.f};
+            for (int kc = 0; kc < 256; kc += 64) {
+                __syncthreads();
+                {
+                    int u = tid;
+                    int r = u >> 4, kq = u & 15;
+                    float4 v = *(const float4*)&P.xc[(size_t)(mb + r) * 256 + kc + kq * 4];
+                    union { ushort u[4]; uint2 v2; } hh, ll;
+                    f2hl(v.x, &hh.u[0], &ll.u[0]); f2hl(v.y, &hh.u[1], &ll.u[1]);
+                    f2hl(v.z, &hh.u[2], &ll.u[2]); f2hl(v.w, &hh.u[3], &ll.u[3]);
+                    *(uint2*)&AsH[r][kq * 4] = hh.v2;
+                    *(uint2*)&AsL[r][kq * 4] = ll.v2;
+                }
+                {
+                    int u = tid;
+                    int n = u >> 3, g = u & 7;
+                    size_t go = (size_t)(W_PROJ) + (size_t)(nb + n) * 256 + kc + g * 8;
+                    *(uint4*)&BsH[n][g * 8] = *(const uint4*)&P.wH[go];
+                    *(uint4*)&BsL[n][g * 8] = *(const uint4*)&P.wL[go];
+                }
+                __syncthreads();
+#pragma unroll
+                for (int ks_ = 0; ks_ < 64; ks_ += 32) {
+                    const int kk = ks_ + q * 8;
+                    bf16x8 ah = *(const bf16x8*)&AsH[wm2 * 16 + ln][kk];
+                    bf16x8 al = *(const bf16x8*)&AsL[wm2 * 16 + ln][kk];
+                    bf16x8 bh = *(const bf16x8*)&BsH[wn4 * 16 + ln][kk];
+                    bf16x8 bl = *(const bf16x8*)&BsL[wn4 * 16 + ln][kk];
+                    acc = __builtin_amdgcn_mfma_f32_16x16x32_bf16(ah, bh, acc, 0, 0, 0);
+                    acc = __builtin_amdgcn_mfma_f32_16x16x32_bf16(ah, bl, acc, 0, 0, 0);
+                    acc = __builtin_amdgcn_mfma_f32_16x16x32_bf16(al, bh, acc, 0, 0, 0);
+                }
+            }
+#pragma unroll
+            for (int r = 0; r < 4; ++r) {
+                int l = mb + wm2 * 16 + q * 4 + r;
+                int col = nb + wn4 * 16 + ln;
+                float v = acc[r];
+                float rho = (float)l * (1.0f / 8191.0f);
+                int band = min(7, (int)(rho * 8.0f));
+                float mv = P.mbuf[l];
+                if (col < 256) {
+                    float sc0 = 2.0f * sigm(P.edt[band] + P.wr[0] * rho + P.wm[0] * mv);
+                    float v2 = v + P.bdt[col];
+                    float sp = (v2 > 20.f) ? v2 : log1pf(expf(v2));
+                    P.dt[(size_t)l * 256 + col] = sp * sc0;
+                } else if (col < 272) {
+                    float sc1 = 2.0f * sigm(P.eB[band] + P.wr[1] * rho + P.wm[1] * mv);
+                    P.Bm[(size_t)l * 16 + (col - 256)] = v * sc1;
+                } else if (col < 288) {
+                    float sc2 = 2.0f * sigm(P.eC[band] + P.wr[2] * rho + P.wm[2] * mv);
+                    P.Cm[(size_t)l * 16 + (col - 272)] = v * sc2;
+                }
+            }
+        }
+    }
+    gg.sync();
+
+    {
+        const int sub = tid >> 8, e = tid & 255;
+        float (*bms)[16] = (float(*)[16])(smem + sub * 2048);
+        const int c = b, dir = sub;
+        for (int idx = e; idx < 512; idx += 256)
+            bms[idx >> 4][idx & 15] = P.Bm[c * 512 + idx];
+        float A2[16], iv[16], h[16];
+#pragma unroll
+        for (int n = 0; n < 16; ++n) {
+            float ea = nexp2(P.Alog[e * 16 + n] * LOG2E);
+            A2[n] = -ea * LOG2E;
+            iv[n] = -1.0f / ea;
+            h[n] = 0.f;
+        }
+        const int base = c * CLh;
+        float cu[8], cx[8], nu[8], nx[8];
+#pragma unroll
+        for (int j = 0; j < 8; ++j) {
+            int p = dir ? (CLh - 1 - j) : j;
+            cu[j] = P.dt[(size_t)(base + p) * 256 + e];
+            cx[j] = P.xc[(size_t)(base + p) * 256 + e];
+        }
         __syncthreads();
-        for (int u = tid; u < 256; u += 256) {
-            int r = u >> 3, g = u & 7;
-            size_t go = (size_t)(mb + r) * 128 + kc + g * 8;
-            *(uint4*)&AsH[r][g * 8] = *(const uint4*)&Ah[go];
-            *(uint4*)&AsL[r][g * 8] = *(const uint4*)&Al[go];
-        }
-        for (int u = tid; u < 512; u += 256) {
-            int n = u >> 3, g = u & 7;
-            size_t go = (size_t)(W_PU) + (size_t)(nb + n) * 128 + kc + g * 8;
-            *(uint4*)&BsH[n][g * 8] = *(const uint4*)&wH[go];
-            *(uint4*)&BsL[n][g * 8] = *(const uint4*)&wL[go];
-        }
+        float sdt = 0.f;
+#pragma unroll
+        for (int g = 0; g < CLh / 8; ++g) {
+            if (g + 1 < CLh / 8) {
+#pragma unroll
+                for (int j = 0; j < 8; ++j) {
+                    int s = (g + 1) * 8 + j;
+                    int p = dir ? (CLh - 1 - s) : s;
+                    nu[j] = P.dt[(size_t)(base + p) * 256 + e];
+                    nx[j] = P.xc[(size_t)(base + p) * 256 + e];
+                }
+            }
+#pragma unroll
+            for (int j = 0; j < 8; ++j) {
+                int s = g * 8 + j;
+                int p = dir ? (CLh - 1 - s) : s;
+                float u = cu[j], xv = cx[j];
+                union { float4 v[4]; float f[16]; } bb;
+                const float4* bp = (const float4*)&bms[p][0];
+                bb.v[0] = bp[0]; bb.v[1] = bp[1]; bb.v[2] = bp[2]; bb.v[3] = bp[3];
+#pragma unroll
+                for (int n = 0; n < 16; ++n) {
+                    float a = nexp2(A2[n] * u);
+                    float w = xv * bb.f[n] * iv[n];
+                    h[n] = a * (h[n] + w) - w;
+                }
+                sdt += u;
+            }
+#pragma unroll
+            for (int j = 0; j < 8; ++j) { cu[j] = nu[j]; cx[j] = nx[j]; }
+        }
+        const size_t hofs = (size_t)(dir * NCh + c) * 4096 + e * 16;
+#pragma unroll
+        for (int j = 0; j < 4; ++j)
+            *(float4*)&P.Hb[hofs + 4 * j] = make_float4(h[4 * j], h[4 * j + 1], h[4 * j + 2], h[4 * j + 3]);
+        if (dir == 0) P.sdtb[c * 256 + e] = sdt;
+    }
+    gg.sync();
+
+    if (gtid < 8192) {
+        int dir = gtid >> 12, en = gtid & 4095, e = en >> 4;
+        float A2 = -nexp2(P.Alog[en] * LOG2E) * LOG2E;
+        float hi = 0.f;
+        for (int g = 0; g < NCh / 8; ++g) {
+            float Pv[8], qv[8];
+#pragma unroll
+            for (int j = 0; j < 8; ++j) {
+                int c = dir ? (NCh - 1 - (g * 8 + j)) : (g * 8 + j);
+                Pv[j] = P.sdtb[c * 256 + e];
+                qv[j] = P.Hb[(size_t)(dir * NCh + c) * 4096 + en];
+            }
+#pragma unroll
+            for (int j = 0; j < 8; ++j) {
+                int c = dir ? (NCh - 1 - (g * 8 + j)) : (g * 8 + j);
+                float Pp = nexp2(A2 * Pv[j]);
+                P.Hpre[(size_t)(dir * NCh + c) * 4096 + en] = hi;
+                hi = Pp * hi + qv[j];
+            }
+        }
+    }
+    gg.sync();
+
+    {
+        const int c = b;
+        const int dir = tid >> 8;
+        const int e = tid & 255;
+        float (*bms)[16] = (float(*)[16])(smem);
+        float (*cms)[16] = (float(*)[16])(smem + 2048);
+        float (*ysum)[256] = (float(*)[256])(smem + 4096);
+        for (int idx = tid; idx < 512; idx += 512) {
+            bms[idx >> 4][idx & 15] = P.Bm[c * 512 + idx];
+            cms[idx >> 4][idx & 15] = P.Cm[c * 512 + idx];
+        }
+        float A2[16], iv[16], h[16];
+#pragma unroll
+        for (int n = 0; n < 16; ++n) {
+            float ea = nexp2(P.Alog[e * 16 + n] * LOG2E);
+            A2[n] = -ea * LOG2E;
+            iv[n] = -1.0f / ea;
+        }
+        const size_t hofs = (size_t)(dir * NCh + c) * 4096 + e * 16;
+#pragma unroll
+        for (int j = 0; j < 4; ++j) {
+            float4 hv = *(const float4*)&P.Hpre[hofs + 4 * j];
+            h[4 * j] = hv.x; h[4 * j + 1] = hv.y; h[4 * j + 2] = hv.z; h[4 * j + 3] = hv.w;
+        }
+        const int base = c * CLh;
+        float yreg[CLh];
         __syncthreads();
-#pragma unroll
-        for (int ks_ = 0; ks_ < 64; ks_ += 32) {
-            const int kk = ks_ + q * 8;
-            bf16x8 ah = *(const bf16x8*)&AsH[wm * 16 + ln][kk];
-            bf16x8 al = *(const bf16x8*)&AsL[wm * 16 + ln][kk];
-#pragma unroll
-            for (int cb = 0; cb < 2; ++cb) {
-                bf16x8 bh = *(const bf16x8*)&BsH[wn * 32 + cb * 16 + ln][kk];
-                bf16x8 bl = *(const bf16x8*)&BsL[wn * 32 + cb * 16 + ln][kk];
-                acc[cb] = __builtin_amdgcn_mfma_f32_16x16x32_bf16(ah, bh, acc[cb], 0, 0, 0);
-                acc[cb] = __builtin_amdgcn_mfma_f32_16x16x32_bf16(ah, bl, acc[cb], 0, 0, 0);
-                acc[cb] = __builtin_amdgcn_mfma_f32_16x16x32_bf16(al, bh, acc[cb], 0, 0, 0);
-            }
-        }
-    }
-#pragma unroll
-    for (int cb = 0; cb < 2; ++cb)
-#pragma unroll
-        for (int r = 0; r < 4; ++r) {
-            int l = mb + wm * 16 + q * 4 + r;
-            int col = nb + wn * 32 + cb * 16 + ln;
-            int xg = l >> 8, yg = (l >> 3) & 31, zg = l & 7;
-            int c = col >> 3, ijk = col & 7;
-            int i2 = (ijk >> 2) & 1, j2 = (ijk >> 1) & 1, k2 = ijk & 1;
-            size_t idx = (size_t)((c * 64 + 2 * xg + i2) * 64 + (2 * yg + j2)) * 16 + 2 * zg + k2;
-            out[idx] = acc[cb][r] + pu_b[c] + ks[idx];
-        }
+        if (dir == 0) {
+            scan_dir<0>(P.dt, P.xc, base, e, bms, cms, A2, iv, h, yreg);
+        } else {
+            scan_dir<1>(P.dt, P.xc, base, e, bms, cms, A2, iv, h, yreg);
+        }
+        __syncthreads();
+        if (dir == 0) {
+#pragma unroll
+            for (int l = 0; l < CLh; ++l) ysum[l][e] = yreg[l];
+        }
+        __syncthreads();
+        if (dir == 1) {
+            float dpv = P.Dp[e];
+#pragma unroll
+            for (int l = 0; l < CLh; ++l) {
+                size_t gl = (size_t)(base + l) * 256 + e;
+                float a = (ysum[l][e] + yreg[l] + dpv * P.xc[gl]) * P.sz[gl];
+                ushort hh, ll; f2hl(a, &hh, &ll);
+                P.AHo[gl] = hh; P.ALo[gl] = ll;
+            }
+        }
+    }
+    gg.sync();
+
+    {
+        const int sub = tid >> 8, st = tid & 255;
+        char* sm = smem + sub * 27648;
+        ushort (*AsH)[72] = (ushort(*)[72])(sm);
+        ushort (*AsL)[72] = (ushort(*)[72])(sm + 4608);
+        ushort (*BsH)[72] = (ushort(*)[72])(sm + 9216);
+        ushort (*BsL)[72] = (ushort(*)[72])(sm + 18432);
+        const int lane = st & 63, wave = st >> 6;
+        const int wm2 = wave & 1, wn2 = wave >> 1;
+        const int ln = lane & 15, q = lane >> 4;
+        const int mb = b * 32, nb = sub * 64;
+        f32x4 acc[2];
+        acc[0] = (f32x4){0.f, 0.f, 0.f, 0.f};
+        acc[1] = (f32x4){0.f, 0.f, 0.f, 0.f};
+        for (int kc = 0; kc < 256; kc += 64) {
+            __syncthreads();
+            {
+                int u = st;
+                int r = u >> 3, g = u & 7;
+                size_t go = (size_t)(mb + r) * 256 + kc + g * 8;
+                *(uint4*)&AsH[r][g * 8] = *(const uint4*)&P.AHo[go];
+                *(uint4*)&AsL[r][g * 8] = *(const uint4*)&P.ALo[go];
+            }
+            for (int u = st; u < 512; u += 256) {
+                int n = u >> 3, g = u & 7;
+                size_t go = (size_t)(W_WOUT) + (size_t)(nb + n) * 256 + kc + g * 8;
+                *(uint4*)&BsH[n][g * 8] = *(const uint4*)&P.wH[go];
+                *(uint4*)&BsL[n][g * 8] = *(const uint4*)&P.wL[go];
+            }
+            __syncthreads();
+#pragma unroll
+            for (int ks_ = 0; ks_ < 64; ks_ += 32) {
+                const int kk = ks_ + q * 8;
+                bf16x8 ah = *(const bf16x8*)&AsH[wm2 * 16 + ln][kk];
+                bf16x8 al = *(const bf16x8*)&AsL[wm2 * 16 + ln][kk];
+#pragma unroll
+                for (int cb = 0; cb < 2; ++cb) {
+                    bf16x8 bh = *(const bf16x8*)&BsH[wn2 * 32 + cb * 16 + ln][kk];
+                    bf16x8 bl = *(const bf16x8*)&BsL[wn2 * 32 + cb * 16 + ln][kk];
+                    acc[cb] = __builtin_amdgcn_mfma_f32_16x16x32_bf16(ah, bh, acc[cb], 0, 0, 0);
+                    acc[cb] = __builtin_amdgcn_mfma_f32_16x16x32_bf16(ah, bl, acc[cb], 0, 0, 0);
+                    acc[cb] = __builtin_amdgcn_mfma_f32_16x16x32_bf16(al, bh, acc[cb], 0, 0, 0);
+                }
+            }
+        }
+#pragma unroll
+        for (int cb = 0; cb < 2; ++cb)
+#pragma unroll
+            for (int r = 0; r < 4; ++r) {
+                int l = mb + wm2 * 16 + q * 4 + r;
+                int col = nb + wn2 * 32 + cb * 16 + ln;
+                float v = acc[cb][r] + P.bout[col] + P.h_[(size_t)l * 128 + col];
+                ushort hh, ll; f2hl(v, &hh, &ll);
+                P.hfH[(size_t)l * 128 + col] = hh;
+                P.hfL[(size_t)l * 128 + col] = ll;
+            }
+    }
+    gg.sync();
+
+    {
+        const int sub = tid >> 8, st = tid & 255;
+        char* sm = smem + sub * 27648;
+        ushort (*AsH)[72] = (ushort(*)[72])(sm);
+        ushort (*AsL)[72] = (ushort(*)[72])(sm + 4608);
+        ushort (*BsH)[72] = (ushort(*)[72])(sm + 9216);
+        ushort (*BsL)[72] = (ushort(*)[72])(sm + 18432);
+        const int lane = st & 63, wave = st >> 6;
+        const int wm2 = wave & 1, wn2 = wave >> 1;
+        const int ln = lane & 15, q = lane >> 4;
+        const int mb = b * 32, nb = sub * 64;
+        f32x4 acc[2];
+        acc[0] = (f32x4){0.f, 0.f, 0.f, 0.f};
+        acc[1] = (f32x4){0.f, 0.f, 0.f, 0.f};
+        for (int kc = 0; kc < 128; kc += 64) {
+            __syncthreads();
+            {
+                int u = st;
+                int r = u >> 3, g = u & 7;
+                size_t go = (size_t)(mb + r) * 128 + kc + g * 8;
+                *(uint4*)&AsH[r][g * 8] = *(const uint4*)&P.hfH[go];
+                *(uint4*)&AsL[r][g * 8] = *(const uint4*)&P.hfL[go];
+            }
+            for (int u = st; u < 512; u += 256) {
+                int n = u >> 3, g = u & 7;
+                size_t go = (size_t)(W_PU) + (size_t)(nb + n) * 128 + kc + g * 8;
+                *(uint4*)&BsH[n][g * 8] = *(const uint4*)&P.wH[go];
+                *(uint4*)&BsL[n][g * 8] = *(const uint4*)&P.wL[go];
+            }
+            __syncthreads();
+#pragma unroll
+            for (int ks_ = 0; ks_ < 64; ks_ += 32) {
+                const int kk = ks_ + q * 8;
+                bf16x8 ah = *(const bf16x8*)&AsH[wm2 * 16 + ln][kk];
+                bf16x8 al = *(const bf16x8*)&AsL[wm2 * 16 + ln][kk];
+#pragma unroll
+                for (int cb = 0; cb < 2; ++cb) {
+                    bf16x8 bh = *(const bf16x8*)&BsH[wn2 * 32 + cb * 16 + ln][kk];
+                    bf16x8 bl = *(const bf16x8*)&BsL[wn2 * 32 + cb * 16 + ln][kk];
+                    acc[cb] = __builtin_amdgcn_mfma_f32_16x16x32_bf16(ah, bh, acc[cb], 0, 0, 0);
+                    acc[cb] = __builtin_amdgcn_mfma_f32_16x16x32_bf16(ah, bl, acc[cb], 0, 0, 0);
+                    acc[cb] = __builtin_amdgcn_mfma_f32_16x16x32_bf16(al, bh, acc[cb], 0, 0, 0);
+                }
+            }
+        }
+#pragma unroll
+        for (int cb = 0; cb < 2; ++cb)
+#pragma unroll
+            for (int r = 0; r < 4; ++r) {
+                int l = mb + wm2 * 16 + q * 4 + r;
+                int col = nb + wn2 * 32 + cb * 16 + ln;
+                int xg = l >> 8, yg = (l >> 3) & 31, zg = l & 7;
+                int cc = col >> 3, ijk = col & 7;
+                int i2 = (ijk >> 2) & 1, j2 = (ijk >> 1) & 1, k2 = ijk & 1;
+                size_t idx = (size_t)((cc * 64 + 2 * xg + i2) * 64 + (2 * yg + j2)) * 16 + 2 * zg + k2;
+                P.out[idx] = acc[cb][r] + P.pu_b[cc] + P.ks[idx];
+            }
+    }
 }
 
 extern "C" void kernel_launch(void* const* d_in, const int* in_sizes, int n_in,
                               void* d_out, int out_size, void* d_ws, size_t ws_size,
                               hipStream_t stream) {
-    const float* ks    = (const float*)d_in[0];
-    const float* mask  = (const float*)d_in[1];
-    const float* pe_w  = (const float*)d_in[2];
-    const float* pe_b  = (const float*)d_in[3];
-    const float* pu_w  = (const float*)d_in[4];
-    const float* pu_b  = (const float*)d_in[5];
-    const float* ln_g  = (const float*)d_in[6];
-    const float* ln_b  = (const float*)d_in[7];
-    const float* fn_g  = (const float*)d_in[8];
-    const float* fn_b  = (const float*)d_in[9];
-    const float* cond_band = (const float*)d_in[10];
-    const float* cond_rad  = (const float*)d_in[11];
-    const float* cond_mask = (const float*)d_in[12];
-    const float* Win   = (const float*)d_in[13];
-    const float* bin_  = (const float*)d_in[14];
-    const float* convw = (const float*)d_in[15];
-    const float* convb = (const float*)d_in[16];
-    const float* Wx    = (const float*)d_in[17];
-    const float* Wdt   = (const float*)d_in[18];
-    const float* bdt   = (const float*)d_in[19];
-    const float* Alog  = (const float*)d_in[20];
-    const float* Dp    = (const float*)d_in[21];
-    const float* Wout  = (const float*)d_in[22];
-    const float* bout  = (const float*)d_in[23];
-    const float* edt   = (const float*)d_in[24];
-    const float* eB    = (const float*)d_in[25];
-    const float* eC    = (const float*)d_in[26];
-    const float* wr    = (const float*)d_in[27];
-    const float* wm    = (const float*)d_in[28];
-    float* out = (float*)d_out;
+    KParams P;
+    P.ks    = (const float*)d_in[0];
+    P.mask  = (const float*)d_in[1];
+    P.pe_w  = (const float*)d_in[2];
+    P.pe_b  = (const float*)d_in[3];
+    P.pu_w  = (const float*)d_in[4];
+    P.pu_b  = (const float*)d_in[5];
+    P.ln_g  = (const float*)d_in[6];
+    P.ln_b  = (const float*)d_in[7];
+    P.fn_g  = (const float*)d_in[8];
+    P.fn_b  = (const float*)d_in[9];
+    P.cond_band = (const float*)d_in[10];
+    P.cond_rad  = (const float*)d_in[11];
+    P.cond_mask = (const float*)d_in[12];
+    P.Win   = (const float*)d_in[13];
+    P.bin_  = (const float*)d_in[14];
+    P.convw = (const float*)d_in[15];
+    P.convb = (const float*)d_in[16];
+    P.Wx    = (const float*)d_in[17];
+    P.Wdt   = (const float*)d_in[18];
+    P.bdt   = (const float*)d_in[19];
+    P.Alog  = (const float*)d_in[20];
+    P.Dp    = (const float*)d_in[21];
+    P.Wout  = (const float*)d_in[22];
+    P.bout  = (const float*)d_in[23];
+    P.edt   = (const float*)d_in[24];
+    P.eB    = (const float*)d_in[25];
+    P.eC    = (const float*)d_in[26];
+    P.wr    = (const float*)d_in[27];
+    P.wm    = (const float*)d_in[28];
+    P.out   = (float*)d_out;
 
     char* base = (char*)d_ws;
     size_t o = 0;
     auto alloc = [&](size_t bytes) { char* p = base + o; o += (bytes + 255) & ~(size_t)255; return p; };
-    float*  mbuf = (float*)alloc(32768);
-    ushort* wH   = (ushort*)alloc(W_TOT * 2);
-    ushort* wL   = (ushort*)alloc(W_TOT * 2);
-    float*  h_   = (float*)alloc(4194304);
-    ushort* hnH  = (ushort*)alloc(2097152);
-    ushort* hnL  = (ushort*)alloc(2097152);
-    float*  xp   = (float*)alloc(8388608);
-    float*  sz   = (float*)alloc(8388608);
-    float*  xc   = (float*)alloc(8388608);
-    float*  dt   = (float*)alloc(8388608);
-    float*  Bm   = (float*)alloc(524288);
-    float*  Cm   = (float*)alloc(524288);
-    float*  Hb   = (float*)alloc(8388608);
-    float*  Hpre = (float*)alloc(8388608);
-    float*  sdtb = (float*)alloc(262144);
-    ushort* AHo  = (ushort*)alloc(4194304);
-    ushort* ALo  = (ushort*)alloc(4194304);
-    ushort* hfH  = (ushort*)alloc(2097152);
-    ushort* hfL  = (ushort*)alloc(2097152);
-
-    prep_k<<<864, 256, 0, stream>>>(pe_w, Win, Wx, Wdt, Wout, pu_w, mask, wH, wL, mbuf);
-    embed_ln_k<<<512, 256, 0, stream>>>(ks, wH, wL, pe_b, cond_band, cond_rad, cond_mask, mbuf,
-                                        ln_g, ln_b, fn_g, fn_b, h_, hnH, hnL);
-    win_k<<<dim3(128, 8), 256, 0, stream>>>(hnH, hnL, wH, wL, bin_, xp, sz);
-    conv_k<<<2048, 256, 0, stream>>>(xp, convw, convb, xc);
-    proj_k<<<dim3(128, 5), 256, 0, stream>>>(xc, wH, wL, bdt, mbuf, edt, eB, eC, wr, wm, dt, Bm, Cm);
-    scan0_k<<<dim3(NCh, 2), 256, 0, stream>>>(dt, xc, Bm, Alog, Hb, sdtb);
-    combine_k<<<128, 64, 0, stream>>>(Hb, Hpre, sdtb, Alog);
-    scan1g_k<<<NCh, 512, 0, stream>>>(dt, xc, Bm, Cm, Alog, Hpre, sz, Dp, AHo, ALo);
-    wout_k<<<dim3(256, 2), 256, 0, stream>>>(AHo, ALo, wH, wL, bout, h_, hfH, hfL);
-    unembed_k<<<dim3(256, 2), 256, 0, stream>>>(hfH, hfL, wH, wL, pu_b, ks, out);
+    P.mbuf = (float*)alloc(32768);
+    P.wH   = (ushort*)alloc(W_TOT * 2);
+    P.wL   = (ushort*)alloc(W_TOT * 2);
+    P.h_   = (float*)alloc(4194304);
+    P.hnH  = (ushort*)alloc(2097152);
+    P.hnL  = (ushort*)alloc(2097152);
+    P.xp   = (float*)alloc(8388608);
+    P.sz   = (float*)alloc(8388608);
+    P.xc   = (float*)alloc(8388608);
+    P.dt   = (float*)alloc(8388608);
+    P.Bm   = (float*)alloc(524288);
+    P.Cm   = (float*)alloc(524288);
+    P.Hb   = (float*)alloc(8388608);
+    P.Hpre = (float*)alloc(8388608);
+    P.sdtb = (float*)alloc(262144);
+    P.AHo  = (ushort*)alloc(4194304);
+    P.ALo  = (ushort*)alloc(4194304);
+    P.hfH  = (ushort*)alloc(2097152);
+    P.hfL  = (ushort*)alloc(2097152);
+
+    void* args[] = { (void*)&P };
+    hipLaunchCooperativeKernel((const void*)mega_k, dim3(256), dim3(512), args, 0, stream);
 }
```

Result: slower. 548.6 us (+128.6%).
